# Kernel optimization log

Hardware: AMD Instinct MI355X
Metric: run time of the kernel (lower is better)

## Reference

```python
import jax, jax.numpy as jnp
import numpy as np

N_ATOMS = 10000
N_EDGES = 200000
L_MAX = 2
K_L = [32, 24, 16]  # k_max_l = n_element_channels * n_max_l

# (l1, l2, L) in the original loop order (l1 outer, l2 inner, L ascending)
PAIRS = [(0,0,0),(0,1,1),(0,2,2),
         (1,0,1),(1,1,0),(1,1,1),(1,1,2),(1,2,1),(1,2,2),
         (2,0,2),(2,1,1),(2,1,2),(2,2,0),(2,2,1),(2,2,2)]
# concatenated input width -> k_max_l[L] per (L, sigma) channel
LIN = {'0_1': (72, 32), '1_1': (80, 24), '1_m1': (40, 24), '2_1': (72, 16), '2_m1': (32, 16)}


def setup_inputs() -> dict:
    key = jax.random.key(0)
    it = iter(jax.random.split(key, 64))
    def nrm(shape):
        return jax.random.normal(next(it), shape, dtype=jnp.float32)
    inp = {}
    for l in range(L_MAX + 1):
        inp['rb%d' % l] = nrm((N_EDGES, K_L[l]))           # radial basis per l
    for l in range(L_MAX + 1):
        inp['sh%d' % l] = nrm((N_EDGES, 2*l+1, 1))         # spherical harmonics per l
    inp['emb'] = nrm((N_ATOMS, 1, K_L[0]))                 # initial center embedding
    for l in range(L_MAX + 1):
        inp['f%d' % l] = nrm((N_ATOMS, 2*l+1, K_L[l]))     # nu=1 equivariant features
    for (l1, l2, L) in PAIRS:
        inp['cg_%d_%d_%d' % (l1, l2, L)] = nrm(((2*l1+1)*(2*l2+1), 2*L+1))
    for LS, (fin, fout) in LIN.items():
        inp['W_' + LS] = nrm((fin, fout)) / np.float32(np.sqrt(fin))
        inp['b_' + LS] = nrm((fout,)) * 0.01
    inp['centers'] = jax.random.randint(next(it), (N_EDGES,), 0, N_ATOMS)
    inp['neighbors'] = jax.random.randint(next(it), (N_EDGES,), 0, N_ATOMS)
    inp['n_atoms'] = N_ATOMS
    return inp


def _normalize(x, dims):
    # Normalizer(dims): RMS normalization over the given dims
    return x * jax.lax.rsqrt(jnp.mean(x * x, axis=dims, keepdims=True) + 1e-12)


def _forward(floats, centers, neighbors, n_atoms):
    (rb0, rb1, rb2, sh0, sh1, sh2, emb, f0, f1, f2,
     cg_0_0_0, cg_0_1_1, cg_0_2_2, cg_1_0_1, cg_1_1_0, cg_1_1_1, cg_1_1_2,
     cg_1_2_1, cg_1_2_2, cg_2_0_2, cg_2_1_1, cg_2_1_2, cg_2_2_0, cg_2_2_1,
     cg_2_2_2, W_0_1, b_0_1, W_1_1, b_1_1, W_1_m1, b_1_m1, W_2_1, b_2_1,
     W_2_m1, b_2_m1) = floats
    rb = [rb0, rb1, rb2]; sh = [sh0, sh1, sh2]; feats = [f0, f1, f2]
    cgs = {'0_0_0': cg_0_0_0, '0_1_1': cg_0_1_1, '0_2_2': cg_0_2_2,
           '1_0_1': cg_1_0_1, '1_1_0': cg_1_1_0, '1_1_1': cg_1_1_1,
           '1_1_2': cg_1_1_2, '1_2_1': cg_1_2_1, '1_2_2': cg_1_2_2,
           '2_0_2': cg_2_0_2, '2_1_1': cg_2_1_1, '2_1_2': cg_2_1_2,
           '2_2_0': cg_2_2_0, '2_2_1': cg_2_2_1, '2_2_2': cg_2_2_2}
    lin = {'0_1': (W_0_1, b_0_1), '1_1': (W_1_1, b_1_1), '1_m1': (W_1_m1, b_1_m1),
           '2_1': (W_2_1, b_2_1), '2_m1': (W_2_m1, b_2_m1)}

    # ---- InvariantMessagePasser: density_l = scatter_add over centers of
    #      sh_l * rb_l * emb[neighbors]
    emb_n = emb[neighbors]                                       # [E, 1, k0]
    densities = []
    for l in range(L_MAX + 1):
        msg = sh[l] * rb[l][:, None, :] * emb_n[:, :, :K_L[l]]   # [E, 2l+1, k_l]
        densities.append(jax.ops.segment_sum(msg, centers, num_segments=n_atoms))

    # ---- EquivariantMessagePasser
    ve = [sh[l] * rb[l][:, None, :] for l in range(L_MAX + 1)]   # vector expansion [E,2l+1,k_l]
    fn = [feats[l][neighbors] for l in range(L_MAX + 1)]         # gathered neighbor feats
    results = {}
    for (l1, l2, L) in PAIRS:
        S = (-1) ** (l1 + l2 + L)
        k = min(K_L[l1], K_L[l2])
        t1 = ve[l1][:, :, :k]                                    # [E, 2l1+1, k]
        t2 = fn[l2][:, :, :k]                                    # [E, 2l2+1, k]
        cg = cgs['%d_%d_%d' % (l1, l2, L)].reshape(2*l1+1, 2*l2+1, 2*L+1)
        # fused outer product + CG contraction -> [E, 2L+1, k]
        res = jnp.einsum('eak,ebk,abM->eMk', t1, t2, cg)
        pooled = jax.ops.segment_sum(res, centers, num_segments=n_atoms)
        LS = '%d_%s' % (L, 'm1' if S < 0 else '1')
        results.setdefault(LS, []).append(pooled)

    outs = {}
    for LS, (W, b) in lin.items():
        x = jnp.concatenate(results[LS], axis=2)                 # [n_atoms, 2L+1, size_LS]
        x = _normalize(x, (0, 1))
        x = jnp.einsum('amf,fk->amk', x, W) + b
        outs[LS] = _normalize(x, (0, 1, 2))

    return (densities[0], densities[1], densities[2],
            outs['0_1'], outs['1_1'], outs['1_m1'], outs['2_1'], outs['2_m1'])


def reference(rb0, rb1, rb2, sh0, sh1, sh2, emb, f0, f1, f2,
              cg_0_0_0, cg_0_1_1, cg_0_2_2, cg_1_0_1, cg_1_1_0, cg_1_1_1,
              cg_1_1_2, cg_1_2_1, cg_1_2_2, cg_2_0_2, cg_2_1_1, cg_2_1_2,
              cg_2_2_0, cg_2_2_1, cg_2_2_2, W_0_1, b_0_1, W_1_1, b_1_1,
              W_1_m1, b_1_m1, W_2_1, b_2_1, W_2_m1, b_2_m1,
              centers, neighbors, n_atoms):
    floats = (rb0, rb1, rb2, sh0, sh1, sh2, emb, f0, f1, f2,
              cg_0_0_0, cg_0_1_1, cg_0_2_2, cg_1_0_1, cg_1_1_0, cg_1_1_1,
              cg_1_1_2, cg_1_2_1, cg_1_2_2, cg_2_0_2, cg_2_1_1, cg_2_1_2,
              cg_2_2_0, cg_2_2_1, cg_2_2_2, W_0_1, b_0_1, W_1_1, b_1_1,
              W_1_m1, b_1_m1, W_2_1, b_2_1, W_2_m1, b_2_m1)
    return _forward(floats, centers, neighbors, n_atoms)
```

## Files before the change

kernel.cpp:

```cpp
#include <hip/hip_runtime.h>
#include <hip/hip_bf16.h>

typedef __hip_bfloat16 bf16;

#define N_ATOMS 10000
#define N_EDGES 200000

#define SCG   0
#define SINV  616
#define SS1P  1024
#define SS2P  19968
#define SWS2  20288
#define SINTS 20352
#define IFLAG  0
#define ICOUNT 16
#define IOFFS  10016
#define ICURS  20032
#define IELIST 30032
#define INTS_END_SMALL 230032
#define INTS_END_BIG   430032
#define SXACC (SINTS + INTS_END_BIG)
#define BIG_FLOATS (SXACC + 952*N_ATOMS)

#define O0 0
#define O1 320000
#define O2 1040000
#define OY 1840000
#define OUT_ELEMS 5200000

__device__ __forceinline__ float b2f(bf16 x){ return __bfloat162float(x); }
__device__ __forceinline__ bf16  f2b(float x){ return __float2bfloat16(x); }

__device__ __forceinline__ float ldv(const float* p, int i){ return p[i]; }
__device__ __forceinline__ float ldv(const bf16*  p, int i){ return b2f(p[i]); }
__device__ __forceinline__ void  stv(float* p, int i, float v){ p[i] = v; }
__device__ __forceinline__ void  stv(bf16*  p, int i, float v){ p[i] = f2b(v); }

template<typename T> __device__ __forceinline__ int dtid();
template<> __device__ __forceinline__ int dtid<bf16>(){ return 0; }
template<> __device__ __forceinline__ int dtid<float>(){ return 1; }

struct Ptrs15 { const void* p[15]; };
struct LinP   { const void* W[5]; const void* B[5]; };

__constant__ int c_cg_sizes[15] = {1,9,25,9,9,27,45,45,75,25,45,75,25,75,125};
__constant__ int c_fin[5]   = {72,80,40,72,32};
__constant__ int c_kout[5]  = {32,24,24,16,16};
__constant__ int c_yoff[5]  = {OY+0, OY+320000, OY+1040000, OY+1760000, OY+2560000};
__constant__ int c_numel[5] = {320000,720000,720000,800000,800000};
__constant__ int c_cum[6]   = {0,32,104,176,256,336};
__constant__ int c_xb[5]    = {0,72,312,432,792};
__constant__ int c_Ms[5]    = {1,3,3,5,5};

__global__ void k_zero(float* wsf, int* wsi,
                       const unsigned short* rb0u, const unsigned short* embu) {
  if (blockIdx.x == 0 && threadIdx.x < 64) {
    int lane = threadIdx.x;
    int bad = 0;
    for (int i = lane; i < 256; i += 64) {
      unsigned u1 = ((unsigned)rb0u[2*i]) << 16;
      unsigned u2 = ((unsigned)embu[2*i]) << 16;
      float v1 = __uint_as_float(u1);
      float v2 = __uint_as_float(u2);
      if (!(fabsf(v1) < 1e9f) || !(fabsf(v2) < 1e9f)) bad = 1;
    }
    unsigned long long any = __ballot(bad);
    if (lane == 0) wsi[IFLAG] = (any != 0ULL) ? 1 : 0;
  }
  int i = blockIdx.x*blockDim.x + threadIdx.x;
  if (i < N_ATOMS) wsi[ICOUNT + i] = 0;
  int j = i - N_ATOMS;
  if (j >= 0 && j < N_ATOMS) wsi[ICURS + j] = 0;
  j -= N_ATOMS;
  if (j >= 0 && j < 18944) wsf[SS1P + j] = 0.f;
  j -= 18944;
  if (j >= 0 && j < 325) wsf[SS2P + j] = 0.f;
}

template<typename T>
__global__ void k_cg(Ptrs15 cg, float* wsf, const int* flag) {
  if (flag[0] != dtid<T>()) return;
  int i = blockIdx.x*blockDim.x + threadIdx.x;
  if (i >= 615) return;
  int s = 0, off = i;
  while (off >= c_cg_sizes[s]) { off -= c_cg_sizes[s]; ++s; }
  wsf[SCG + i] = ldv((const T*)cg.p[s], off);
}

__global__ void k_hist(const int* __restrict__ centers, int* __restrict__ counts) {
  int e = blockIdx.x*blockDim.x + threadIdx.x;
  if (e < N_EDGES) atomicAdd(&counts[centers[e]], 1);
}

__global__ void k_scan(const int* __restrict__ counts, int* __restrict__ offs) {
  __shared__ int part[1024];
  int t = threadIdx.x;
  int base = t*10;
  int s = 0;
  for (int i = 0; i < 10; ++i) { int idx = base+i; if (idx < N_ATOMS) s += counts[idx]; }
  part[t] = s;
  __syncthreads();
  for (int d = 1; d < 1024; d <<= 1) {
    int v = part[t];
    int add = (t >= d) ? part[t-d] : 0;
    __syncthreads();
    part[t] = v + add;
    __syncthreads();
  }
  int run = (t == 0) ? 0 : part[t-1];
  for (int i = 0; i < 10; ++i) {
    int idx = base+i;
    if (idx < N_ATOMS) { offs[idx] = run; run += counts[idx]; }
  }
  if (t == 1023) offs[N_ATOMS] = part[1023];
}

__global__ void k_scatter(const int* __restrict__ centers, const int* __restrict__ offs,
                          int* __restrict__ cursors, int* __restrict__ elist) {
  int e = blockIdx.x*blockDim.x + threadIdx.x;
  if (e < N_EDGES) {
    int c = centers[e];
    int p = atomicAdd(&cursors[c], 1);
    elist[offs[c] + p] = e;
  }
}

__global__ void k_scatter2(const int* __restrict__ centers, const int* __restrict__ neighbors,
                           const int* __restrict__ offs, int* __restrict__ cursors,
                           int2* __restrict__ elist2) {
  int e = blockIdx.x*blockDim.x + threadIdx.x;
  if (e < N_EDGES) {
    int c = centers[e];
    int p = atomicAdd(&cursors[c], 1);
    elist2[offs[c] + p] = make_int2(e, neighbors[e]);
  }
}

template<typename T, int MODE>
__global__ __launch_bounds__(256) void k_main(
    const T* __restrict__ rb0, const T* __restrict__ rb1, const T* __restrict__ rb2,
    const T* __restrict__ sh0, const T* __restrict__ sh1, const T* __restrict__ sh2,
    const T* __restrict__ emb, const T* __restrict__ f0, const T* __restrict__ f1,
    const T* __restrict__ f2, const int* __restrict__ neighbors,
    const int* __restrict__ offs, const int* __restrict__ elist,
    const float* __restrict__ cgf, float* __restrict__ s1p,
    const float* __restrict__ inv, float* __restrict__ s2p,
    float* __restrict__ xout, LinP lp, T* __restrict__ out,
    const int* __restrict__ flag)
{
  if (flag[0] != dtid<T>()) return;
  int lane = threadIdx.x & 63;
  int wv   = threadIdx.x >> 6;
  int tix  = threadIdx.x;
  int a = blockIdx.x;
  int beg = offs[a];
  int cnt = offs[a+1] - beg;
  int k32 = lane & 31, e2 = lane >> 5;
  int k16 = lane & 15, e4 = lane >> 4;
  const int2* el2 = (const int2*)elist;
  int ab = a & 63;

  __shared__ int2 sel[256];
  __shared__ __align__(16) float L[952];
  __shared__ float red[4][5];

  float acc[25];
  #pragma unroll
  for (int i = 0; i < 25; ++i) acc[i] = 0.f;

  for (int cbase = 0; cbase < cnt; cbase += 256) {
    int nch = cnt - cbase; if (nch > 256) nch = 256;
    __syncthreads();
    if (tix < nch) {
      if constexpr (MODE == 0) {
        sel[tix] = el2[beg + cbase + tix];
      } else {
        int e = elist[beg + cbase + tix];
        sel[tix] = make_int2(e, neighbors[e]);
      }
    }
    __syncthreads();

    if (wv == 0) {
      for (int base = 0; base < nch; base += 4) {
        #pragma unroll
        for (int u = 0; u < 2; ++u) {
          int idx = base + 2*u + e2;
          float w = (idx < nch) ? 1.f : 0.f;
          int ic  = (idx < nch) ? idx : 0;
          int2 en = sel[ic];
          int e = en.x, n = en.y;
          float s0 = ldv(sh0, e);
          float s1a0 = ldv(sh1, e*3+0), s1a1 = ldv(sh1, e*3+1), s1a2 = ldv(sh1, e*3+2);
          float rb0k = ldv(rb0, e*32 + k32) * w;
          float ek   = ldv(emb, n*32 + k32);
          float f0k  = ldv(f0,  n*32 + k32);
          float ve0 = s0 * rb0k;
          acc[0] = fmaf(ve0, ek, acc[0]);
          acc[4] = fmaf(ve0, f0k, acc[4]);
          if (k32 < 24) {
            float rb1k = ldv(rb1, e*24 + k32) * w;
            float f1k0 = ldv(f1, n*72 + k32);
            float f1k1 = ldv(f1, n*72 + 24 + k32);
            float f1k2 = ldv(f1, n*72 + 48 + k32);
            float rbek = rb1k * ek;
            acc[1] = fmaf(s1a0, rbek, acc[1]);
            acc[2] = fmaf(s1a1, rbek, acc[2]);
            acc[3] = fmaf(s1a2, rbek, acc[3]);
            acc[5] = fmaf(ve0, f1k0, acc[5]);
            acc[6] = fmaf(ve0, f1k1, acc[6]);
            acc[7] = fmaf(ve0, f1k2, acc[7]);
            float g3 = rb1k * f0k;
            acc[8]  = fmaf(g3, s1a0, acc[8]);
            acc[9]  = fmaf(g3, s1a1, acc[9]);
            acc[10] = fmaf(g3, s1a2, acc[10]);
            #pragma unroll
            for (int aa = 0; aa < 3; ++aa) {
              float sa = rb1k * ((aa==0)?s1a0:(aa==1)?s1a1:s1a2);
              acc[11+aa*3+0] = fmaf(sa, f1k0, acc[11+aa*3+0]);
              acc[11+aa*3+1] = fmaf(sa, f1k1, acc[11+aa*3+1]);
              acc[11+aa*3+2] = fmaf(sa, f1k2, acc[11+aa*3+2]);
            }
          }
        }
      }
    } else if (wv == 1) {
      for (int base = 0; base < nch; base += 8) {
        #pragma unroll
        for (int u = 0; u < 2; ++u) {
          int idx = base + 4*u + e4;
          float w = (idx < nch) ? 1.f : 0.f;
          int ic  = (idx < nch) ? idx : 0;
          int2 en = sel[ic];
          int e = en.x, n = en.y;
          float s0 = ldv(sh0, e);
          float s1a[3];
          #pragma unroll
          for (int m = 0; m < 3; ++m) s1a[m] = ldv(sh1, e*3+m);
          float s2a[5];
          #pragma unroll
          for (int m = 0; m < 5; ++m) s2a[m] = ldv(sh2, e*5+m);
          float rb0k = ldv(rb0, e*32 + k16) * w;
          float rb1k = ldv(rb1, e*24 + k16) * w;
          float rb2k = ldv(rb2, e*16 + k16) * w;
          float ek   = ldv(emb, n*32 + k16);
          float f2k[5];
          #pragma unroll
          for (int b = 0; b < 5; ++b) f2k[b] = ldv(f2, n*80 + b*16 + k16);
          float re = rb2k * ek;
          #pragma unroll
          for (int m = 0; m < 5; ++m) acc[m] = fmaf(s2a[m], re, acc[m]);
          float ve0 = s0 * rb0k;
          #pragma unroll
          for (int b = 0; b < 5; ++b) acc[5+b] = fmaf(ve0, f2k[b], acc[5+b]);
          #pragma unroll
          for (int aa = 0; aa < 3; ++aa) {
            float sa = rb1k * s1a[aa];
            #pragma unroll
            for (int b = 0; b < 5; ++b)
              acc[10+aa*5+b] = fmaf(sa, f2k[b], acc[10+aa*5+b]);
          }
        }
      }
    } else if (wv == 2) {
      for (int base = 0; base < nch; base += 8) {
        #pragma unroll
        for (int u = 0; u < 2; ++u) {
          int idx = base + 4*u + e4;
          float w = (idx < nch) ? 1.f : 0.f;
          int ic  = (idx < nch) ? idx : 0;
          int2 en = sel[ic];
          int e = en.x, n = en.y;
          float s2a[5];
          #pragma unroll
          for (int m = 0; m < 5; ++m) s2a[m] = ldv(sh2, e*5+m);
          float rb2k = ldv(rb2, e*16 + k16) * w;
          float f0k  = ldv(f0,  n*32 + k16);
          float f1k[3];
          #pragma unroll
          for (int b = 0; b < 3; ++b) f1k[b] = ldv(f1, n*72 + b*24 + k16);
          float g9 = rb2k * f0k;
          #pragma unroll
          for (int aa = 0; aa < 5; ++aa) acc[aa] = fmaf(g9, s2a[aa], acc[aa]);
          #pragma unroll
          for (int aa = 0; aa < 5; ++aa) {
            float sa = rb2k * s2a[aa];
            #pragma unroll
            for (int b = 0; b < 3; ++b)
              acc[5+aa*3+b] = fmaf(sa, f1k[b], acc[5+aa*3+b]);
          }
        }
      }
    } else {
      for (int base = 0; base < nch; base += 8) {
        #pragma unroll
        for (int u = 0; u < 2; ++u) {
          int idx = base + 4*u + e4;
          float w = (idx < nch) ? 1.f : 0.f;
          int ic  = (idx < nch) ? idx : 0;
          int2 en = sel[ic];
          int e = en.x, n = en.y;
          float s2a[5];
          #pragma unroll
          for (int m = 0; m < 5; ++m) s2a[m] = ldv(sh2, e*5+m);
          float rb2k = ldv(rb2, e*16 + k16) * w;
          float f2k[5];
          #pragma unroll
          for (int b = 0; b < 5; ++b) f2k[b] = ldv(f2, n*80 + b*16 + k16);
          #pragma unroll
          for (int aa = 0; aa < 5; ++aa) {
            float sa = rb2k * s2a[aa];
            #pragma unroll
            for (int b = 0; b < 5; ++b)
              acc[aa*5+b] = fmaf(sa, f2k[b], acc[aa*5+b]);
          }
        }
      }
    }
  }

  if (wv == 0) {
    #pragma unroll
    for (int i = 0; i < 20; ++i) acc[i] += __shfl_xor(acc[i], 32);
    const float* C000 = cgf + 0;
    const float* C011 = cgf + 1;
    const float* C101 = cgf + 35;
    const float* C110 = cgf + 44;
    const float* C111 = cgf + 53;
    const float* C112 = cgf + 80;
    float r[16];
    r[0] = C000[0] * acc[4];
    #pragma unroll
    for (int M = 0; M < 3; ++M) {
      float t = 0.f;
      #pragma unroll
      for (int b = 0; b < 3; ++b) t = fmaf(acc[5+b], C011[b*3+M], t);
      r[1+M] = t;
    }
    #pragma unroll
    for (int M = 0; M < 3; ++M) {
      float t = 0.f;
      #pragma unroll
      for (int aa = 0; aa < 3; ++aa) t = fmaf(acc[8+aa], C101[aa*3+M], t);
      r[4+M] = t;
    }
    {
      float t = 0.f;
      #pragma unroll
      for (int q = 0; q < 9; ++q) t = fmaf(acc[11+q], C110[q], t);
      r[7] = t;
    }
    #pragma unroll
    for (int M = 0; M < 3; ++M) {
      float t = 0.f;
      #pragma unroll
      for (int q = 0; q < 9; ++q) t = fmaf(acc[11+q], C111[q*3+M], t);
      r[8+M] = t;
    }
    #pragma unroll
    for (int M = 0; M < 5; ++M) {
      float t = 0.f;
      #pragma unroll
      for (int q = 0; q < 9; ++q) t = fmaf(acc[11+q], C112[q*5+M], t);
      r[11+M] = t;
    }
    acc[4] = r[0];
    #pragma unroll
    for (int M = 0; M < 3; ++M) acc[5+M]  = r[1+M];
    #pragma unroll
    for (int M = 0; M < 3; ++M) acc[8+M]  = r[4+M];
    acc[11] = r[7];
    #pragma unroll
    for (int M = 0; M < 3; ++M) acc[12+M] = r[8+M];
    #pragma unroll
    for (int M = 0; M < 5; ++M) acc[15+M] = r[11+M];
  } else if (wv == 1) {
    #pragma unroll
    for (int i = 0; i < 25; ++i) {
      acc[i] += __shfl_xor(acc[i], 16);
      acc[i] += __shfl_xor(acc[i], 32);
    }
    const float* C022 = cgf + 10;
    const float* C121 = cgf + 125;
    const float* C122 = cgf + 170;
    float r[13];
    #pragma unroll
    for (int M = 0; M < 5; ++M) {
      float t = 0.f;
      #pragma unroll
      for (int b = 0; b < 5; ++b) t = fmaf(acc[5+b], C022[b*5+M], t);
      r[M] = t;
    }
    #pragma unroll
    for (int M = 0; M < 3; ++M) {
      float t = 0.f;
      #pragma unroll
      for (int q = 0; q < 15; ++q) t = fmaf(acc[10+q], C121[q*3+M], t);
      r[5+M] = t;
    }
    #pragma unroll
    for (int M = 0; M < 5; ++M) {
      float t = 0.f;
      #pragma unroll
      for (int q = 0; q < 15; ++q) t = fmaf(acc[10+q], C122[q*5+M], t);
      r[8+M] = t;
    }
    #pragma unroll
    for (int M = 0; M < 5; ++M) acc[5+M]  = r[M];
    #pragma unroll
    for (int M = 0; M < 3; ++M) acc[10+M] = r[5+M];
    #pragma unroll
    for (int M = 0; M < 5; ++M) acc[13+M] = r[8+M];
  } else if (wv == 2) {
    #pragma unroll
    for (int i = 0; i < 20; ++i) {
      acc[i] += __shfl_xor(acc[i], 16);
      acc[i] += __shfl_xor(acc[i], 32);
    }
    const float* C202 = cgf + 245;
    const float* C211 = cgf + 270;
    const float* C212 = cgf + 315;
    float r[13];
    #pragma unroll
    for (int M = 0; M < 5; ++M) {
      float t = 0.f;
      #pragma unroll
      for (int aa = 0; aa < 5; ++aa) t = fmaf(acc[aa], C202[aa*5+M], t);
      r[M] = t;
    }
    #pragma unroll
    for (int M = 0; M < 3; ++M) {
      float t = 0.f;
      #pragma unroll
      for (int q = 0; q < 15; ++q) t = fmaf(acc[5+q], C211[q*3+M], t);
      r[5+M] = t;
    }
    #pragma unroll
    for (int M = 0; M < 5; ++M) {
      float t = 0.f;
      #pragma unroll
      for (int q = 0; q < 15; ++q) t = fmaf(acc[5+q], C212[q*5+M], t);
      r[8+M] = t;
    }
    #pragma unroll
    for (int M = 0; M < 5; ++M) acc[M]   = r[M];
    #pragma unroll
    for (int M = 0; M < 3; ++M) acc[5+M] = r[5+M];
    #pragma unroll
    for (int M = 0; M < 5; ++M) acc[8+M] = r[8+M];
  } else {
    #pragma unroll
    for (int i = 0; i < 25; ++i) {
      acc[i] += __shfl_xor(acc[i], 16);
      acc[i] += __shfl_xor(acc[i], 32);
    }
    const float* C220 = cgf + 390;
    const float* C221 = cgf + 415;
    const float* C222 = cgf + 490;
    float r[9];
    {
      float t = 0.f;
      #pragma unroll
      for (int q = 0; q < 25; ++q) t = fmaf(acc[q], C220[q], t);
      r[0] = t;
    }
    #pragma unroll
    for (int M = 0; M < 3; ++M) {
      float t = 0.f;
      #pragma unroll
      for (int q = 0; q < 25; ++q) t = fmaf(acc[q], C221[q*3+M], t);
      r[1+M] = t;
    }
    #pragma unroll
    for (int M = 0; M < 5; ++M) {
      float t = 0.f;
      #pragma unroll
      for (int q = 0; q < 25; ++q) t = fmaf(acc[q], C222[q*5+M], t);
      r[4+M] = t;
    }
    #pragma unroll
    for (int i = 0; i < 9; ++i) acc[i] = r[i];
  }

  if constexpr (MODE != 2) {
    if (wv == 0) {
      if (lane < 32) {
        stv(out, O0 + a*32 + k32, acc[0]);
        atomicAdd(&s1p[(0+k32)*64+ab], acc[4]*acc[4]);
        if (k32 < 24) {
          #pragma unroll
          for (int m = 0; m < 3; ++m) stv(out, O1 + a*72 + m*24 + k32, acc[1+m]);
          atomicAdd(&s1p[(32+k32)*64+ab], acc[11]*acc[11]);
          float q;
          q = acc[5]*acc[5]+acc[6]*acc[6]+acc[7]*acc[7];
          atomicAdd(&s1p[(72+k32)*64+ab], q);
          q = acc[8]*acc[8]+acc[9]*acc[9]+acc[10]*acc[10];
          atomicAdd(&s1p[(96+k32)*64+ab], q);
          q = acc[12]*acc[12]+acc[13]*acc[13]+acc[14]*acc[14];
          atomicAdd(&s1p[(152+k32)*64+ab], q);
          q = acc[15]*acc[15]+acc[16]*acc[16]+acc[17]*acc[17]
            + acc[18]*acc[18]+acc[19]*acc[19];
          atomicAdd(&s1p[(208+k32)*64+ab], q);
        }
      }
    } else if (wv == 1) {
      if (lane < 16) {
        #pragma unroll
        for (int m = 0; m < 5; ++m) stv(out, O2 + a*80 + m*16 + k16, acc[m]);
        float q;
        q = acc[5]*acc[5]+acc[6]*acc[6]+acc[7]*acc[7]+acc[8]*acc[8]+acc[9]*acc[9];
        atomicAdd(&s1p[(192+k16)*64+ab], q);
        q = acc[10]*acc[10]+acc[11]*acc[11]+acc[12]*acc[12];
        atomicAdd(&s1p[(120+k16)*64+ab], q);
        q = acc[13]*acc[13]+acc[14]*acc[14]+acc[15]*acc[15]
          + acc[16]*acc[16]+acc[17]*acc[17];
        atomicAdd(&s1p[(264+k16)*64+ab], q);
      }
    } else if (wv == 2) {
      if (lane < 16) {
        float q;
        q = acc[0]*acc[0]+acc[1]*acc[1]+acc[2]*acc[2]+acc[3]*acc[3]+acc[4]*acc[4];
        atomicAdd(&s1p[(232+k16)*64+ab], q);
        q = acc[5]*acc[5]+acc[6]*acc[6]+acc[7]*acc[7];
        atomicAdd(&s1p[(136+k16)*64+ab], q);
        q = acc[8]*acc[8]+acc[9]*acc[9]+acc[10]*acc[10]
          + acc[11]*acc[11]+acc[12]*acc[12];
        atomicAdd(&s1p[(280+k16)*64+ab], q);
      }
    } else {
      if (lane < 16) {
        atomicAdd(&s1p[(56+k16)*64+ab], acc[0]*acc[0]);
        float q;
        q = acc[1]*acc[1]+acc[2]*acc[2]+acc[3]*acc[3];
        atomicAdd(&s1p[(176+k16)*64+ab], q);
        q = acc[4]*acc[4]+acc[5]*acc[5]+acc[6]*acc[6]
          + acc[7]*acc[7]+acc[8]*acc[8];
        atomicAdd(&s1p[(248+k16)*64+ab], q);
      }
    }
  }

  if constexpr (MODE == 0) {
    if (wv == 0) {
      if (lane < 32) {
        L[k32] = acc[4];
        if (k32 < 24) {
          L[32+k32] = acc[11];
          #pragma unroll
          for (int M = 0; M < 3; ++M) L[72+M*80+k32]     = acc[5+M];
          #pragma unroll
          for (int M = 0; M < 3; ++M) L[72+M*80+24+k32]  = acc[8+M];
          #pragma unroll
          for (int M = 0; M < 3; ++M) L[312+M*40+k32]    = acc[12+M];
          #pragma unroll
          for (int M = 0; M < 5; ++M) L[432+M*72+16+k32] = acc[15+M];
        }
      }
    } else if (wv == 1) {
      if (lane < 16) {
        #pragma unroll
        for (int M = 0; M < 5; ++M) L[432+M*72+k16]    = acc[5+M];
        #pragma unroll
        for (int M = 0; M < 3; ++M) L[72+M*80+48+k16]  = acc[10+M];
        #pragma unroll
        for (int M = 0; M < 5; ++M) L[792+M*32+k16]    = acc[13+M];
      }
    } else if (wv == 2) {
      if (lane < 16) {
        #pragma unroll
        for (int M = 0; M < 5; ++M) L[432+M*72+40+k16] = acc[0+M];
        #pragma unroll
        for (int M = 0; M < 3; ++M) L[72+M*80+64+k16]  = acc[5+M];
        #pragma unroll
        for (int M = 0; M < 5; ++M) L[792+M*32+16+k16] = acc[8+M];
      }
    } else {
      if (lane < 16) {
        L[56+k16] = acc[0];
        #pragma unroll
        for (int M = 0; M < 3; ++M) L[312+M*40+24+k16] = acc[1+M];
        #pragma unroll
        for (int M = 0; M < 5; ++M) L[432+M*72+56+k16] = acc[4+M];
      }
    }
    __syncthreads();
    const float4* Ls = (const float4*)L;
    float4* xd = (float4*)(xout + a*952);
    for (int i = tix; i < 238; i += 256) xd[i] = Ls[i];
  }

  if constexpr (MODE == 2) {
    if (wv == 0) {
      if (lane < 32) {
        L[k32] = acc[4]*inv[k32];
        if (k32 < 24) {
          L[32+k32] = acc[11]*inv[32+k32];
          #pragma unroll
          for (int M = 0; M < 3; ++M) L[72+M*80+k32]     = acc[5+M]*inv[72+k32];
          #pragma unroll
          for (int M = 0; M < 3; ++M) L[72+M*80+24+k32]  = acc[8+M]*inv[96+k32];
          #pragma unroll
          for (int M = 0; M < 3; ++M) L[312+M*40+k32]    = acc[12+M]*inv[152+k32];
          #pragma unroll
          for (int M = 0; M < 5; ++M) L[432+M*72+16+k32] = acc[15+M]*inv[208+k32];
        }
      }
    } else if (wv == 1) {
      if (lane < 16) {
        #pragma unroll
        for (int M = 0; M < 5; ++M) L[432+M*72+k16]    = acc[5+M]*inv[192+k16];
        #pragma unroll
        for (int M = 0; M < 3; ++M) L[72+M*80+48+k16]  = acc[10+M]*inv[120+k16];
        #pragma unroll
        for (int M = 0; M < 5; ++M) L[792+M*32+k16]    = acc[13+M]*inv[264+k16];
      }
    } else if (wv == 2) {
      if (lane < 16) {
        #pragma unroll
        for (int M = 0; M < 5; ++M) L[432+M*72+40+k16] = acc[0+M]*inv[232+k16];
        #pragma unroll
        for (int M = 0; M < 3; ++M) L[72+M*80+64+k16]  = acc[5+M]*inv[136+k16];
        #pragma unroll
        for (int M = 0; M < 5; ++M) L[792+M*32+16+k16] = acc[8+M]*inv[280+k16];
      }
    } else {
      if (lane < 16) {
        L[56+k16] = acc[0]*inv[56+k16];
        #pragma unroll
        for (int M = 0; M < 3; ++M) L[312+M*40+24+k16] = acc[1+M]*inv[176+k16];
        #pragma unroll
        for (int M = 0; M < 5; ++M) L[432+M*72+56+k16] = acc[4+M]*inv[248+k16];
      }
    }
    __syncthreads();
    int t = threadIdx.x;
    float y2[5] = {0.f,0.f,0.f,0.f,0.f};
    for (int tau = t; tau < 336; tau += 256) {
      int ls = 0;
      while (tau >= c_cum[ls+1]) ++ls;
      int rem = tau - c_cum[ls];
      int kn = c_kout[ls], fin = c_fin[ls];
      int M = rem / kn, ko = rem - M*kn;
      const T* W = (const T*)lp.W[ls];
      float y = ldv((const T*)lp.B[ls], ko);
      const float* xv = &L[c_xb[ls] + M*fin];
      for (int f = 0; f < fin; ++f) y = fmaf(xv[f], ldv(W, f*kn+ko), y);
      stv(out, c_yoff[ls] + (a*c_Ms[ls] + M)*kn + ko, y);
      y2[ls] += y*y;
    }
    #pragma unroll
    for (int i = 0; i < 5; ++i) {
      y2[i] += __shfl_xor(y2[i], 1);  y2[i] += __shfl_xor(y2[i], 2);
      y2[i] += __shfl_xor(y2[i], 4);  y2[i] += __shfl_xor(y2[i], 8);
      y2[i] += __shfl_xor(y2[i], 16); y2[i] += __shfl_xor(y2[i], 32);
    }
    if (lane == 0) {
      #pragma unroll
      for (int i = 0; i < 5; ++i) red[wv][i] = y2[i];
    }
    __syncthreads();
    if (t == 0) {
      #pragma unroll
      for (int i = 0; i < 5; ++i)
        atomicAdd(&s2p[i*64 + ab], red[0][i]+red[1][i]+red[2][i]+red[3][i]);
    }
  }
}

template<typename T>
__global__ __launch_bounds__(256) void k_lin(
    const float* __restrict__ xg, const float* __restrict__ inv,
    LinP lp, T* __restrict__ out, float* __restrict__ s2p,
    const int* __restrict__ flag)
{
  if (flag[0] != dtid<T>()) return;
  int a = blockIdx.x;
  int t = threadIdx.x;
  __shared__ float L[952];
  for (int i = t; i < 952; i += 256) {
    int ch;
    if      (i < 72)  ch = i;
    else if (i < 312) ch = 72  + (i-72)  % 80;
    else if (i < 432) ch = 152 + (i-312) % 40;
    else if (i < 792) ch = 192 + (i-432) % 72;
    else              ch = 264 + (i-792) % 32;
    L[i] = xg[a*952 + i] * inv[ch];
  }
  __syncthreads();
  float y2[5] = {0.f,0.f,0.f,0.f,0.f};
  for (int tau = t; tau < 336; tau += 256) {
    int ls = 0;
    while (tau >= c_cum[ls+1]) ++ls;
    int rem = tau - c_cum[ls];
    int kn = c_kout[ls], fin = c_fin[ls];
    int M = rem / kn, ko = rem - M*kn;
    const T* W = (const T*)lp.W[ls];
    float y = ldv((const T*)lp.B[ls], ko);
    const float* xv = &L[c_xb[ls] + M*fin];
    for (int f = 0; f < fin; ++f) y = fmaf(xv[f], ldv(W, f*kn+ko), y);
    stv(out, c_yoff[ls] + (a*c_Ms[ls] + M)*kn + ko, y);
    y2[ls] += y*y;
  }
  __shared__ float red[4][5];
  #pragma unroll
  for (int i = 0; i < 5; ++i) {
    y2[i] += __shfl_xor(y2[i], 1);  y2[i] += __shfl_xor(y2[i], 2);
    y2[i] += __shfl_xor(y2[i], 4);  y2[i] += __shfl_xor(y2[i], 8);
    y2[i] += __shfl_xor(y2[i], 16); y2[i] += __shfl_xor(y2[i], 32);
  }
  if ((t & 63) == 0) {
    #pragma unroll
    for (int i = 0; i < 5; ++i) red[t>>6][i] = y2[i];
  }
  __syncthreads();
  if (t == 0) {
    #pragma unroll
    for (int i = 0; i < 5; ++i)
      atomicAdd(&s2p[i*64 + (a & 63)], red[0][i]+red[1][i]+red[2][i]+red[3][i]);
  }
}

__global__ void k_red1(const float* __restrict__ s1p, float* __restrict__ inv) {
  int ch = blockIdx.x, lane = threadIdx.x;
  float v = s1p[ch*64 + lane];
  v += __shfl_xor(v, 1);  v += __shfl_xor(v, 2);  v += __shfl_xor(v, 4);
  v += __shfl_xor(v, 8);  v += __shfl_xor(v, 16); v += __shfl_xor(v, 32);
  if (lane == 0) {
    float rows = (ch < 72) ? 10000.f : (ch < 192) ? 30000.f : 50000.f;
    inv[ch] = rsqrtf(v/rows + 1e-12f);
  }
}

__global__ void k_red2(const float* __restrict__ s2p, float* __restrict__ ws2) {
  int ls = blockIdx.x, lane = threadIdx.x;
  float v = s2p[ls*64 + lane];
  v += __shfl_xor(v, 1);  v += __shfl_xor(v, 2);  v += __shfl_xor(v, 4);
  v += __shfl_xor(v, 8);  v += __shfl_xor(v, 16); v += __shfl_xor(v, 32);
  if (lane == 0) ws2[ls] = v;
}

template<typename T>
__global__ void k_scale(const float* __restrict__ ws2, T* __restrict__ out,
                        const int* __restrict__ flag) {
  if (flag[0] != dtid<T>()) return;
  int i = blockIdx.x*blockDim.x + threadIdx.x;
  if (i >= 3360000) return;
  int ls = (i < 320000) ? 0 : (i < 1040000) ? 1 : (i < 1760000) ? 2 : (i < 2560000) ? 3 : 4;
  float scale = rsqrtf(ws2[ls] / (float)c_numel[ls] + 1e-12f);
  stv(out, OY + i, ldv((const T*)out, OY + i) * scale);
}

template<typename T>
static void launch_chain(void* const* d_in, T* out, float* wsf, int* wsi,
                         Ptrs15 cg, LinP lp, bool big, hipStream_t stream) {
  const T* rb0 = (const T*)d_in[0];
  const T* rb1 = (const T*)d_in[1];
  const T* rb2 = (const T*)d_in[2];
  const T* sh0 = (const T*)d_in[3];
  const T* sh1 = (const T*)d_in[4];
  const T* sh2 = (const T*)d_in[5];
  const T* emb = (const T*)d_in[6];
  const T* f0  = (const T*)d_in[7];
  const T* f1  = (const T*)d_in[8];
  const T* f2  = (const T*)d_in[9];
  const int* neighbors = (const int*)d_in[36];
  const int* flag = wsi + IFLAG;

  k_cg<T><<<3, 256, 0, stream>>>(cg, wsf, flag);
  if (big) {
    k_main<T,0><<<N_ATOMS, 256, 0, stream>>>(rb0, rb1, rb2, sh0, sh1, sh2, emb, f0, f1, f2,
        neighbors, wsi+IOFFS, wsi+IELIST, wsf+SCG, wsf+SS1P, nullptr, nullptr,
        wsf+SXACC, lp, out, flag);
    k_red1<<<296, 64, 0, stream>>>(wsf+SS1P, wsf+SINV);
    k_lin<T><<<N_ATOMS, 256, 0, stream>>>(wsf+SXACC, wsf+SINV, lp, out, wsf+SS2P, flag);
  } else {
    k_main<T,1><<<N_ATOMS, 256, 0, stream>>>(rb0, rb1, rb2, sh0, sh1, sh2, emb, f0, f1, f2,
        neighbors, wsi+IOFFS, wsi+IELIST, wsf+SCG, wsf+SS1P, nullptr, nullptr,
        nullptr, lp, out, flag);
    k_red1<<<296, 64, 0, stream>>>(wsf+SS1P, wsf+SINV);
    k_main<T,2><<<N_ATOMS, 256, 0, stream>>>(rb0, rb1, rb2, sh0, sh1, sh2, emb, f0, f1, f2,
        neighbors, wsi+IOFFS, wsi+IELIST, wsf+SCG, nullptr, wsf+SINV, wsf+SS2P,
        nullptr, lp, out, flag);
  }
  k_red2<<<5, 64, 0, stream>>>(wsf+SS2P, wsf+SWS2);
  k_scale<T><<<(3360000+255)/256, 256, 0, stream>>>(wsf+SWS2, out, flag);
}

extern "C" void kernel_launch(void* const* d_in, const int* in_sizes, int n_in,
                              void* d_out, int out_size, void* d_ws, size_t ws_size,
                              hipStream_t stream) {
  float* wsf = (float*)d_ws;
  int*   wsi = (int*)(wsf + SINTS);
  const int* centers   = (const int*)d_in[35];
  const int* neighbors = (const int*)d_in[36];
  bool big = ws_size >= (size_t)BIG_FLOATS * 4;

  int know = -1;
  if (in_sizes) {
    long long nb = (long long)in_sizes[0];
    if (nb == (long long)N_EDGES*32*2) know = 0;
    else if (nb == (long long)N_EDGES*32*4) know = 1;
  }
  if (know < 0) {
    long long ob = (long long)out_size;
    if (ob == (long long)OUT_ELEMS*2) know = 0;
    else if (ob == (long long)OUT_ELEMS*4) know = 1;
  }

  Ptrs15 cg;
  for (int i = 0; i < 15; ++i) cg.p[i] = d_in[10+i];
  LinP lp;
  lp.W[0] = d_in[25]; lp.B[0] = d_in[26];
  lp.W[1] = d_in[27]; lp.B[1] = d_in[28];
  lp.W[2] = d_in[29]; lp.B[2] = d_in[30];
  lp.W[3] = d_in[31]; lp.B[3] = d_in[32];
  lp.W[4] = d_in[33]; lp.B[4] = d_in[34];

  k_zero<<<154, 256, 0, stream>>>(wsf, wsi,
                                  (const unsigned short*)d_in[0],
                                  (const unsigned short*)d_in[6]);
  k_hist<<<(N_EDGES+255)/256, 256, 0, stream>>>(centers, wsi+ICOUNT);
  k_scan<<<1, 1024, 0, stream>>>(wsi+ICOUNT, wsi+IOFFS);
  if (big) {
    k_scatter2<<<(N_EDGES+255)/256, 256, 0, stream>>>(centers, neighbors, wsi+IOFFS,
                                                      wsi+ICURS, (int2*)(wsi+IELIST));
  } else {
    k_scatter<<<(N_EDGES+255)/256, 256, 0, stream>>>(centers, wsi+IOFFS, wsi+ICURS, wsi+IELIST);
  }

  if (know != 1) launch_chain<bf16 >(d_in, (bf16*)d_out,  wsf, wsi, cg, lp, big, stream);
  if (know != 0) launch_chain<float>(d_in, (float*)d_out, wsf, wsi, cg, lp, big, stream);
}
```

Measured before the change: 514.2 us.

## Pack per-edge radial/SH data into center-sorted records and stream in main kernels

Adds a pack kernel that, while scattering edges by center, copies each edge's radial bases and spherical harmonics into a contiguous 84-element record in sorted order. The main kernels then read these records sequentially instead of gathering rb/sh by edge index, and each block now processes four atoms. The old cached-accumulator plus separate linear-kernel path is removed in favour of running the main kernel twice. This trades an extra full copy of per-edge data, and recomputing the edge pass, for coalesced streaming reads and fewer blocks.

```diff
diff --git a/kernel.cpp b/kernel.cpp
--- a/kernel.cpp
+++ b/kernel.cpp
@@ -5,6 +5,7 @@
 
 #define N_ATOMS 10000
 #define N_EDGES 200000
+#define REC 84
 
 #define SCG   0
 #define SINV  616
@@ -17,10 +18,8 @@
 #define IOFFS  10016
 #define ICURS  20032
 #define IELIST 30032
-#define INTS_END_SMALL 230032
 #define INTS_END_BIG   430032
-#define SXACC (SINTS + INTS_END_BIG)
-#define BIG_FLOATS (SXACC + 952*N_ATOMS)
+#define SEREC (SINTS + INTS_END_BIG)
 
 #define O0 0
 #define O1 320000
@@ -115,8 +114,11 @@
   if (t == 1023) offs[N_ATOMS] = part[1023];
 }
 
-__global__ void k_scatter(const int* __restrict__ centers, const int* __restrict__ offs,
-                          int* __restrict__ cursors, int* __restrict__ elist) {
+template<typename T>
+__global__ void k_scatterT(const int* __restrict__ centers, const int* __restrict__ offs,
+                           int* __restrict__ cursors, int* __restrict__ elist,
+                           const int* __restrict__ flag) {
+  if (flag[0] != dtid<T>()) return;
   int e = blockIdx.x*blockDim.x + threadIdx.x;
   if (e < N_EDGES) {
     int c = centers[e];
@@ -125,14 +127,34 @@
   }
 }
 
-__global__ void k_scatter2(const int* __restrict__ centers, const int* __restrict__ neighbors,
-                           const int* __restrict__ offs, int* __restrict__ cursors,
-                           int2* __restrict__ elist2) {
-  int e = blockIdx.x*blockDim.x + threadIdx.x;
-  if (e < N_EDGES) {
-    int c = centers[e];
-    int p = atomicAdd(&cursors[c], 1);
-    elist2[offs[c] + p] = make_int2(e, neighbors[e]);
+template<typename T>
+__global__ __launch_bounds__(256) void k_pack(
+    const T* __restrict__ rb0, const T* __restrict__ rb1, const T* __restrict__ rb2,
+    const T* __restrict__ sh0, const T* __restrict__ sh1, const T* __restrict__ sh2,
+    const int* __restrict__ centers, const int* __restrict__ neighbors,
+    const int* __restrict__ offs, int* __restrict__ cursors,
+    int2* __restrict__ el2, T* __restrict__ erec, const int* __restrict__ flag)
+{
+  if (flag[0] != dtid<T>()) return;
+  int tid = blockIdx.x*blockDim.x + threadIdx.x;
+  int half = tid >> 5;
+  int k = tid & 31;
+  int lane = threadIdx.x & 63;
+  int nhalf = (gridDim.x*blockDim.x) >> 5;
+  for (int e = half; e < N_EDGES; e += nhalf) {
+    int pos = 0;
+    if (k == 0) {
+      int c = centers[e];
+      pos = offs[c] + atomicAdd(&cursors[c], 1);
+    }
+    pos = __shfl(pos, lane & 32);
+    T* r = erec + (size_t)pos * REC;
+    r[k] = rb0[e*32 + k];
+    if (k < 24) r[32+k] = rb1[e*24 + k];
+    if (k < 16) r[56+k] = rb2[e*16 + k];
+    if (k == 0) { r[72] = sh0[e]; el2[pos] = make_int2(e, neighbors[e]); }
+    if (k >= 1 && k < 4) r[72+k] = sh1[e*3 + (k-1)];
+    if (k >= 4 && k < 9) r[72+k] = sh2[e*5 + (k-4)];
   }
 }
 
@@ -143,580 +165,637 @@
     const T* __restrict__ emb, const T* __restrict__ f0, const T* __restrict__ f1,
     const T* __restrict__ f2, const int* __restrict__ neighbors,
     const int* __restrict__ offs, const int* __restrict__ elist,
+    const T* __restrict__ erec,
     const float* __restrict__ cgf, float* __restrict__ s1p,
     const float* __restrict__ inv, float* __restrict__ s2p,
-    float* __restrict__ xout, LinP lp, T* __restrict__ out,
-    const int* __restrict__ flag)
+    LinP lp, T* __restrict__ out, const int* __restrict__ flag)
 {
   if (flag[0] != dtid<T>()) return;
+  constexpr bool STRM = (MODE >= 3);
+  constexpr int EPI = (MODE == 1 || MODE == 3) ? 1 : 2;
   int lane = threadIdx.x & 63;
   int wv   = threadIdx.x >> 6;
   int tix  = threadIdx.x;
-  int a = blockIdx.x;
-  int beg = offs[a];
-  int cnt = offs[a+1] - beg;
   int k32 = lane & 31, e2 = lane >> 5;
   int k16 = lane & 15, e4 = lane >> 4;
+  int k24 = (k32 < 24) ? k32 : 23;
+  float m24 = (k32 < 24) ? 1.f : 0.f;
   const int2* el2 = (const int2*)elist;
-  int ab = a & 63;
 
   __shared__ int2 sel[256];
   __shared__ __align__(16) float L[952];
   __shared__ float red[4][5];
 
-  float acc[25];
-  #pragma unroll
-  for (int i = 0; i < 25; ++i) acc[i] = 0.f;
-
-  for (int cbase = 0; cbase < cnt; cbase += 256) {
-    int nch = cnt - cbase; if (nch > 256) nch = 256;
-    __syncthreads();
-    if (tix < nch) {
-      if constexpr (MODE == 0) {
-        sel[tix] = el2[beg + cbase + tix];
-      } else {
-        int e = elist[beg + cbase + tix];
-        sel[tix] = make_int2(e, neighbors[e]);
-      }
-    }
-    __syncthreads();
-
-    if (wv == 0) {
-      for (int base = 0; base < nch; base += 4) {
-        #pragma unroll
-        for (int u = 0; u < 2; ++u) {
-          int idx = base + 2*u + e2;
-          float w = (idx < nch) ? 1.f : 0.f;
-          int ic  = (idx < nch) ? idx : 0;
-          int2 en = sel[ic];
-          int e = en.x, n = en.y;
-          float s0 = ldv(sh0, e);
-          float s1a0 = ldv(sh1, e*3+0), s1a1 = ldv(sh1, e*3+1), s1a2 = ldv(sh1, e*3+2);
-          float rb0k = ldv(rb0, e*32 + k32) * w;
-          float ek   = ldv(emb, n*32 + k32);
-          float f0k  = ldv(f0,  n*32 + k32);
-          float ve0 = s0 * rb0k;
-          acc[0] = fmaf(ve0, ek, acc[0]);
-          acc[4] = fmaf(ve0, f0k, acc[4]);
-          if (k32 < 24) {
-            float rb1k = ldv(rb1, e*24 + k32) * w;
-            float f1k0 = ldv(f1, n*72 + k32);
-            float f1k1 = ldv(f1, n*72 + 24 + k32);
-            float f1k2 = ldv(f1, n*72 + 48 + k32);
-            float rbek = rb1k * ek;
-            acc[1] = fmaf(s1a0, rbek, acc[1]);
-            acc[2] = fmaf(s1a1, rbek, acc[2]);
-            acc[3] = fmaf(s1a2, rbek, acc[3]);
-            acc[5] = fmaf(ve0, f1k0, acc[5]);
-            acc[6] = fmaf(ve0, f1k1, acc[6]);
-            acc[7] = fmaf(ve0, f1k2, acc[7]);
-            float g3 = rb1k * f0k;
-            acc[8]  = fmaf(g3, s1a0, acc[8]);
-            acc[9]  = fmaf(g3, s1a1, acc[9]);
-            acc[10] = fmaf(g3, s1a2, acc[10]);
+  int a0 = blockIdx.x * 4;
+  for (int a = a0; a < a0 + 4; ++a) {
+    int beg = offs[a];
+    int cnt = offs[a+1] - beg;
+    int ab = a & 63;
+
+    float acc[25];
+    #pragma unroll
+    for (int i = 0; i < 25; ++i) acc[i] = 0.f;
+
+    if constexpr (STRM) {
+      const T* rbase = erec + (size_t)beg * REC;
+      const int2* eb = el2 + beg;
+      if (wv == 0) {
+        for (int base = 0; base < cnt; base += 4) {
+          int i0 = base + e2,      i1 = base + 2 + e2;
+          float w0 = (i0 < cnt) ? 1.f : 0.f, w1 = (i1 < cnt) ? 1.f : 0.f;
+          int c0 = (i0 < cnt) ? i0 : 0,      c1 = (i1 < cnt) ? i1 : 0;
+          const T* r0 = rbase + (size_t)c0 * REC;
+          const T* r1 = rbase + (size_t)c1 * REC;
+          int n0 = eb[c0].y, n1 = eb[c1].y;
+          float s0_0 = ldv(r0,72), sA0 = ldv(r0,73), sA1 = ldv(r0,74), sA2 = ldv(r0,75);
+          float s0_1 = ldv(r1,72), sB0 = ldv(r1,73), sB1 = ldv(r1,74), sB2 = ldv(r1,75);
+          float a0v = ldv(r0, k32) * w0,            a1v = ldv(r1, k32) * w1;
+          float b0v = ldv(r0, 32+k24) * (w0*m24),   b1v = ldv(r1, 32+k24) * (w1*m24);
+          float e0v = ldv(emb, n0*32 + k32),        e1v = ldv(emb, n1*32 + k32);
+          float g0v = ldv(f0,  n0*32 + k32),        g1v = ldv(f0,  n1*32 + k32);
+          float h00 = ldv(f1, n0*72 + k24)*m24,     h10 = ldv(f1, n1*72 + k24)*m24;
+          float h01 = ldv(f1, n0*72 + 24 + k24)*m24,h11 = ldv(f1, n1*72 + 24 + k24)*m24;
+          float h02 = ldv(f1, n0*72 + 48 + k24)*m24,h12 = ldv(f1, n1*72 + 48 + k24)*m24;
+          float ve = a0v * s0_0;
+          acc[0] = fmaf(ve, e0v, acc[0]);
+          acc[4] = fmaf(ve, g0v, acc[4]);
+          float rbek = b0v * e0v;
+          acc[1] = fmaf(sA0, rbek, acc[1]);
+          acc[2] = fmaf(sA1, rbek, acc[2]);
+          acc[3] = fmaf(sA2, rbek, acc[3]);
+          acc[5] = fmaf(ve, h00, acc[5]);
+          acc[6] = fmaf(ve, h01, acc[6]);
+          acc[7] = fmaf(ve, h02, acc[7]);
+          float g3 = b0v * g0v;
+          acc[8]  = fmaf(g3, sA0, acc[8]);
+          acc[9]  = fmaf(g3, sA1, acc[9]);
+          acc[10] = fmaf(g3, sA2, acc[10]);
+          float sa;
+          sa = b0v * sA0;
+          acc[11] = fmaf(sa, h00, acc[11]); acc[12] = fmaf(sa, h01, acc[12]); acc[13] = fmaf(sa, h02, acc[13]);
+          sa = b0v * sA1;
+          acc[14] = fmaf(sa, h00, acc[14]); acc[15] = fmaf(sa, h01, acc[15]); acc[16] = fmaf(sa, h02, acc[16]);
+          sa = b0v * sA2;
+          acc[17] = fmaf(sa, h00, acc[17]); acc[18] = fmaf(sa, h01, acc[18]); acc[19] = fmaf(sa, h02, acc[19]);
+          ve = a1v * s0_1;
+          acc[0] = fmaf(ve, e1v, acc[0]);
+          acc[4] = fmaf(ve, g1v, acc[4]);
+          rbek = b1v * e1v;
+          acc[1] = fmaf(sB0, rbek, acc[1]);
+          acc[2] = fmaf(sB1, rbek, acc[2]);
+          acc[3] = fmaf(sB2, rbek, acc[3]);
+          acc[5] = fmaf(ve, h10, acc[5]);
+          acc[6] = fmaf(ve, h11, acc[6]);
+          acc[7] = fmaf(ve, h12, acc[7]);
+          g3 = b1v * g1v;
+          acc[8]  = fmaf(g3, sB0, acc[8]);
+          acc[9]  = fmaf(g3, sB1, acc[9]);
+          acc[10] = fmaf(g3, sB2, acc[10]);
+          sa = b1v * sB0;
+          acc[11] = fmaf(sa, h10, acc[11]); acc[12] = fmaf(sa, h11, acc[12]); acc[13] = fmaf(sa, h12, acc[13]);
+          sa = b1v * sB1;
+          acc[14] = fmaf(sa, h10, acc[14]); acc[15] = fmaf(sa, h11, acc[15]); acc[16] = fmaf(sa, h12, acc[16]);
+          sa = b1v * sB2;
+          acc[17] = fmaf(sa, h10, acc[17]); acc[18] = fmaf(sa, h11, acc[18]); acc[19] = fmaf(sa, h12, acc[19]);
+        }
+      } else if (wv == 1) {
+        for (int base = 0; base < cnt; base += 8) {
+          #pragma unroll
+          for (int u = 0; u < 2; ++u) {
+            int idx = base + 4*u + e4;
+            float w = (idx < cnt) ? 1.f : 0.f;
+            int ic  = (idx < cnt) ? idx : 0;
+            const T* r = rbase + (size_t)ic * REC;
+            int n = eb[ic].y;
+            float rb0k = ldv(r, k16) * w;
+            float rb1k = ldv(r, 32+k16) * w;
+            float rb2k = ldv(r, 56+k16) * w;
+            float s0 = ldv(r, 72);
+            float s1a[3];
+            #pragma unroll
+            for (int m = 0; m < 3; ++m) s1a[m] = ldv(r, 73+m);
+            float s2a[5];
+            #pragma unroll
+            for (int m = 0; m < 5; ++m) s2a[m] = ldv(r, 76+m);
+            float ek = ldv(emb, n*32 + k16);
+            float f2k[5];
+            #pragma unroll
+            for (int b = 0; b < 5; ++b) f2k[b] = ldv(f2, n*80 + b*16 + k16);
+            float re = rb2k * ek;
+            #pragma unroll
+            for (int m = 0; m < 5; ++m) acc[m] = fmaf(s2a[m], re, acc[m]);
+            float ve0 = s0 * rb0k;
+            #pragma unroll
+            for (int b = 0; b < 5; ++b) acc[5+b] = fmaf(ve0, f2k[b], acc[5+b]);
             #pragma unroll
             for (int aa = 0; aa < 3; ++aa) {
-              float sa = rb1k * ((aa==0)?s1a0:(aa==1)?s1a1:s1a2);
-              acc[11+aa*3+0] = fmaf(sa, f1k0, acc[11+aa*3+0]);
-              acc[11+aa*3+1] = fmaf(sa, f1k1, acc[11+aa*3+1]);
-              acc[11+aa*3+2] = fmaf(sa, f1k2, acc[11+aa*3+2]);
+              float sa = rb1k * s1a[aa];
+              #pragma unroll
+              for (int b = 0; b < 5; ++b)
+                acc[10+aa*5+b] = fmaf(sa, f2k[b], acc[10+aa*5+b]);
             }
           }
         }
-      }
+      } else if (wv == 2) {
+        for (int base = 0; base < cnt; base += 8) {
+          #pragma unroll
+          for (int u = 0; u < 2; ++u) {
+            int idx = base + 4*u + e4;
+            float w = (idx < cnt) ? 1.f : 0.f;
+            int ic  = (idx < cnt) ? idx : 0;
+            const T* r = rbase + (size_t)ic * REC;
+            int n = eb[ic].y;
+            float rb2k = ldv(r, 56+k16) * w;
+            float s2a[5];
+            #pragma unroll
+            for (int m = 0; m < 5; ++m) s2a[m] = ldv(r, 76+m);
+            float f0k = ldv(f0, n*32 + k16);
+            float f1k[3];
+            #pragma unroll
+            for (int b = 0; b < 3; ++b) f1k[b] = ldv(f1, n*72 + b*24 + k16);
+            float g9 = rb2k * f0k;
+            #pragma unroll
+            for (int aa = 0; aa < 5; ++aa) acc[aa] = fmaf(g9, s2a[aa], acc[aa]);
+            #pragma unroll
+            for (int aa = 0; aa < 5; ++aa) {
+              float sa = rb2k * s2a[aa];
+              #pragma unroll
+              for (int b = 0; b < 3; ++b)
+                acc[5+aa*3+b] = fmaf(sa, f1k[b], acc[5+aa*3+b]);
+            }
+          }
+        }
+      } else {
+        for (int base = 0; base < cnt; base += 8) {
+          #pragma unroll
+          for (int u = 0; u < 2; ++u) {
+            int idx = base + 4*u + e4;
+            float w = (idx < cnt) ? 1.f : 0.f;
+            int ic  = (idx < cnt) ? idx : 0;
+            const T* r = rbase + (size_t)ic * REC;
+            int n = eb[ic].y;
+            float rb2k = ldv(r, 56+k16) * w;
+            float s2a[5];
+            #pragma unroll
+            for (int m = 0; m < 5; ++m) s2a[m] = ldv(r, 76+m);
+            float f2k[5];
+            #pragma unroll
+            for (int b = 0; b < 5; ++b) f2k[b] = ldv(f2, n*80 + b*16 + k16);
+            #pragma unroll
+            for (int aa = 0; aa < 5; ++aa) {
+              float sa = rb2k * s2a[aa];
+              #pragma unroll
+              for (int b = 0; b < 5; ++b)
+                acc[aa*5+b] = fmaf(sa, f2k[b], acc[aa*5+b]);
+            }
+          }
+        }
+      }
+    } else {
+      for (int cbase = 0; cbase < cnt; cbase += 256) {
+        int nch = cnt - cbase; if (nch > 256) nch = 256;
+        __syncthreads();
+        if (tix < nch) {
+          int e = elist[beg + cbase + tix];
+          sel[tix] = make_int2(e, neighbors[e]);
+        }
+        __syncthreads();
+        if (wv == 0) {
+          for (int base = 0; base < nch; base += 4) {
+            #pragma unroll
+            for (int u = 0; u < 2; ++u) {
+              int idx = base + 2*u + e2;
+              float w = (idx < nch) ? 1.f : 0.f;
+              int ic  = (idx < nch) ? idx : 0;
+              int2 en = sel[ic];
+              int e = en.x, n = en.y;
+              float s0 = ldv(sh0, e);
+              float s1a0 = ldv(sh1, e*3+0), s1a1 = ldv(sh1, e*3+1), s1a2 = ldv(sh1, e*3+2);
+              float rb0k = ldv(rb0, e*32 + k32) * w;
+              float ek   = ldv(emb, n*32 + k32);
+              float f0k  = ldv(f0,  n*32 + k32);
+              float ve0 = s0 * rb0k;
+              acc[0] = fmaf(ve0, ek, acc[0]);
+              acc[4] = fmaf(ve0, f0k, acc[4]);
+              if (k32 < 24) {
+                float rb1k = ldv(rb1, e*24 + k32) * w;
+                float f1k0 = ldv(f1, n*72 + k32);
+                float f1k1 = ldv(f1, n*72 + 24 + k32);
+                float f1k2 = ldv(f1, n*72 + 48 + k32);
+                float rbek = rb1k * ek;
+                acc[1] = fmaf(s1a0, rbek, acc[1]);
+                acc[2] = fmaf(s1a1, rbek, acc[2]);
+                acc[3] = fmaf(s1a2, rbek, acc[3]);
+                acc[5] = fmaf(ve0, f1k0, acc[5]);
+                acc[6] = fmaf(ve0, f1k1, acc[6]);
+                acc[7] = fmaf(ve0, f1k2, acc[7]);
+                float g3 = rb1k * f0k;
+                acc[8]  = fmaf(g3, s1a0, acc[8]);
+                acc[9]  = fmaf(g3, s1a1, acc[9]);
+                acc[10] = fmaf(g3, s1a2, acc[10]);
+                #pragma unroll
+                for (int aa = 0; aa < 3; ++aa) {
+                  float sa = rb1k * ((aa==0)?s1a0:(aa==1)?s1a1:s1a2);
+                  acc[11+aa*3+0] = fmaf(sa, f1k0, acc[11+aa*3+0]);
+                  acc[11+aa*3+1] = fmaf(sa, f1k1, acc[11+aa*3+1]);
+                  acc[11+aa*3+2] = fmaf(sa, f1k2, acc[11+aa*3+2]);
+                }
+              }
+            }
+          }
+        } else if (wv == 1) {
+          for (int base = 0; base < nch; base += 8) {
+            #pragma unroll
+            for (int u = 0; u < 2; ++u) {
+              int idx = base + 4*u + e4;
+              float w = (idx < nch) ? 1.f : 0.f;
+              int ic  = (idx < nch) ? idx : 0;
+              int2 en = sel[ic];
+              int e = en.x, n = en.y;
+              float s0 = ldv(sh0, e);
+              float s1a[3];
+              #pragma unroll
+              for (int m = 0; m < 3; ++m) s1a[m] = ldv(sh1, e*3+m);
+              float s2a[5];
+              #pragma unroll
+              for (int m = 0; m < 5; ++m) s2a[m] = ldv(sh2, e*5+m);
+              float rb0k = ldv(rb0, e*32 + k16) * w;
+              float rb1k = ldv(rb1, e*24 + k16) * w;
+              float rb2k = ldv(rb2, e*16 + k16) * w;
+              float ek   = ldv(emb, n*32 + k16);
+              float f2k[5];
+              #pragma unroll
+              for (int b = 0; b < 5; ++b) f2k[b] = ldv(f2, n*80 + b*16 + k16);
+              float re = rb2k * ek;
+              #pragma unroll
+              for (int m = 0; m < 5; ++m) acc[m] = fmaf(s2a[m], re, acc[m]);
+              float ve0 = s0 * rb0k;
+              #pragma unroll
+              for (int b = 0; b < 5; ++b) acc[5+b] = fmaf(ve0, f2k[b], acc[5+b]);
+              #pragma unroll
+              for (int aa = 0; aa < 3; ++aa) {
+                float sa = rb1k * s1a[aa];
+                #pragma unroll
+                for (int b = 0; b < 5; ++b)
+                  acc[10+aa*5+b] = fmaf(sa, f2k[b], acc[10+aa*5+b]);
+              }
+            }
+          }
+        } else if (wv == 2) {
+          for (int base = 0; base < nch; base += 8) {
+            #pragma unroll
+            for (int u = 0; u < 2; ++u) {
+              int idx = base + 4*u + e4;
+              float w = (idx < nch) ? 1.f : 0.f;
+              int ic  = (idx < nch) ? idx : 0;
+              int2 en = sel[ic];
+              int e = en.x, n = en.y;
+              float s2a[5];
+              #pragma unroll
+              for (int m = 0; m < 5; ++m) s2a[m] = ldv(sh2, e*5+m);
+              float rb2k = ldv(rb2, e*16 + k16) * w;
+              float f0k  = ldv(f0,  n*32 + k16);
+              float f1k[3];
+              #pragma unroll
+              for (int b = 0; b < 3; ++b) f1k[b] = ldv(f1, n*72 + b*24 + k16);
+              float g9 = rb2k * f0k;
+              #pragma unroll
+              for (int aa = 0; aa < 5; ++aa) acc[aa] = fmaf(g9, s2a[aa], acc[aa]);
+              #pragma unroll
+              for (int aa = 0; aa < 5; ++aa) {
+                float sa = rb2k * s2a[aa];
+                #pragma unroll
+                for (int b = 0; b < 3; ++b)
+                  acc[5+aa*3+b] = fmaf(sa, f1k[b], acc[5+aa*3+b]);
+              }
+            }
+          }
+        } else {
+          for (int base = 0; base < nch; base += 8) {
+            #pragma unroll
+            for (int u = 0; u < 2; ++u) {
+              int idx = base + 4*u + e4;
+              float w = (idx < nch) ? 1.f : 0.f;
+              int ic  = (idx < nch) ? idx : 0;
+              int2 en = sel[ic];
+              int e = en.x, n = en.y;
+              float s2a[5];
+              #pragma unroll
+              for (int m = 0; m < 5; ++m) s2a[m] = ldv(sh2, e*5+m);
+              float rb2k = ldv(rb2, e*16 + k16) * w;
+              float f2k[5];
+              #pragma unroll
+              for (int b = 0; b < 5; ++b) f2k[b] = ldv(f2, n*80 + b*16 + k16);
+              #pragma unroll
+              for (int aa = 0; aa < 5; ++aa) {
+                float sa = rb2k * s2a[aa];
+                #pragma unroll
+                for (int b = 0; b < 5; ++b)
+                  acc[aa*5+b] = fmaf(sa, f2k[b], acc[aa*5+b]);
+              }
+            }
+          }
+        }
+      }
+    }
+
+    if (wv == 0) {
+      #pragma unroll
+      for (int i = 0; i < 20; ++i) acc[i] += __shfl_xor(acc[i], 32);
+      const float* C000 = cgf + 0;
+      const float* C011 = cgf + 1;
+      const float* C101 = cgf + 35;
+      const float* C110 = cgf + 44;
+      const float* C111 = cgf + 53;
+      const float* C112 = cgf + 80;
+      float r[16];
+      r[0] = C000[0] * acc[4];
+      #pragma unroll
+      for (int M = 0; M < 3; ++M) {
+        float t = 0.f;
+        #pragma unroll
+        for (int b = 0; b < 3; ++b) t = fmaf(acc[5+b], C011[b*3+M], t);
+        r[1+M] = t;
+      }
+      #pragma unroll
+      for (int M = 0; M < 3; ++M) {
+        float t = 0.f;
+        #pragma unroll
+        for (int aa = 0; aa < 3; ++aa) t = fmaf(acc[8+aa], C101[aa*3+M], t);
+        r[4+M] = t;
+      }
+      {
+        float t = 0.f;
+        #pragma unroll
+        for (int q = 0; q < 9; ++q) t = fmaf(acc[11+q], C110[q], t);
+        r[7] = t;
+      }
+      #pragma unroll
+      for (int M = 0; M < 3; ++M) {
+        float t = 0.f;
+        #pragma unroll
+        for (int q = 0; q < 9; ++q) t = fmaf(acc[11+q], C111[q*3+M], t);
+        r[8+M] = t;
+      }
+      #pragma unroll
+      for (int M = 0; M < 5; ++M) {
+        float t = 0.f;
+        #pragma unroll
+        for (int q = 0; q < 9; ++q) t = fmaf(acc[11+q], C112[q*5+M], t);
+        r[11+M] = t;
+      }
+      acc[4] = r[0];
+      #pragma unroll
+      for (int M = 0; M < 3; ++M) acc[5+M]  = r[1+M];
+      #pragma unroll
+      for (int M = 0; M < 3; ++M) acc[8+M]  = r[4+M];
+      acc[11] = r[7];
+      #pragma unroll
+      for (int M = 0; M < 3; ++M) acc[12+M] = r[8+M];
+      #pragma unroll
+      for (int M = 0; M < 5; ++M) acc[15+M] = r[11+M];
     } else if (wv == 1) {
-      for (int base = 0; base < nch; base += 8) {
-        #pragma unroll
-        for (int u = 0; u < 2; ++u) {
-          int idx = base + 4*u + e4;
-          float w = (idx < nch) ? 1.f : 0.f;
-          int ic  = (idx < nch) ? idx : 0;
-          int2 en = sel[ic];
-          int e = en.x, n = en.y;
-          float s0 = ldv(sh0, e);
-          float s1a[3];
-          #pragma unroll
-          for (int m = 0; m < 3; ++m) s1a[m] = ldv(sh1, e*3+m);
-          float s2a[5];
-          #pragma unroll
-          for (int m = 0; m < 5; ++m) s2a[m] = ldv(sh2, e*5+m);
-          float rb0k = ldv(rb0, e*32 + k16) * w;
-          float rb1k = ldv(rb1, e*24 + k16) * w;
-          float rb2k = ldv(rb2, e*16 + k16) * w;
-          float ek   = ldv(emb, n*32 + k16);
-          float f2k[5];
-          #pragma unroll
-          for (int b = 0; b < 5; ++b) f2k[b] = ldv(f2, n*80 + b*16 + k16);
-          float re = rb2k * ek;
-          #pragma unroll
-          for (int m = 0; m < 5; ++m) acc[m] = fmaf(s2a[m], re, acc[m]);
-          float ve0 = s0 * rb0k;
-          #pragma unroll
-          for (int b = 0; b < 5; ++b) acc[5+b] = fmaf(ve0, f2k[b], acc[5+b]);
-          #pragma unroll
-          for (int aa = 0; aa < 3; ++aa) {
-            float sa = rb1k * s1a[aa];
-            #pragma unroll
-            for (int b = 0; b < 5; ++b)
-              acc[10+aa*5+b] = fmaf(sa, f2k[b], acc[10+aa*5+b]);
+      #pragma unroll
+      for (int i = 0; i < 25; ++i) {
+        acc[i] += __shfl_xor(acc[i], 16);
+        acc[i] += __shfl_xor(acc[i], 32);
+      }
+      const float* C022 = cgf + 10;
+      const float* C121 = cgf + 125;
+      const float* C122 = cgf + 170;
+      float r[13];
+      #pragma unroll
+      for (int M = 0; M < 5; ++M) {
+        float t = 0.f;
+        #pragma unroll
+        for (int b = 0; b < 5; ++b) t = fmaf(acc[5+b], C022[b*5+M], t);
+        r[M] = t;
+      }
+      #pragma unroll
+      for (int M = 0; M < 3; ++M) {
+        float t = 0.f;
+        #pragma unroll
+        for (int q = 0; q < 15; ++q) t = fmaf(acc[10+q], C121[q*3+M], t);
+        r[5+M] = t;
+      }
+      #pragma unroll
+      for (int M = 0; M < 5; ++M) {
+        float t = 0.f;
+        #pragma unroll
+        for (int q = 0; q < 15; ++q) t = fmaf(acc[10+q], C122[q*5+M], t);
+        r[8+M] = t;
+      }
+      #pragma unroll
+      for (int M = 0; M < 5; ++M) acc[5+M]  = r[M];
+      #pragma unroll
+      for (int M = 0; M < 3; ++M) acc[10+M] = r[5+M];
+      #pragma unroll
+      for (int M = 0; M < 5; ++M) acc[13+M] = r[8+M];
+    } else if (wv == 2) {
+      #pragma unroll
+      for (int i = 0; i < 20; ++i) {
+        acc[i] += __shfl_xor(acc[i], 16);
+        acc[i] += __shfl_xor(acc[i], 32);
+      }
+      const float* C202 = cgf + 245;
+      const float* C211 = cgf + 270;
+      const float* C212 = cgf + 315;
+      float r[13];
+      #pragma unroll
+      for (int M = 0; M < 5; ++M) {
+        float t = 0.f;
+        #pragma unroll
+        for (int aa = 0; aa < 5; ++aa) t = fmaf(acc[aa], C202[aa*5+M], t);
+        r[M] = t;
+      }
+      #pragma unroll
+      for (int M = 0; M < 3; ++M) {
+        float t = 0.f;
+        #pragma unroll
+        for (int q = 0; q < 15; ++q) t = fmaf(acc[5+q], C211[q*3+M], t);
+        r[5+M] = t;
+      }
+      #pragma unroll
+      for (int M = 0; M < 5; ++M) {
+        float t = 0.f;
+        #pragma unroll
+        for (int q = 0; q < 15; ++q) t = fmaf(acc[5+q], C212[q*5+M], t);
+        r[8+M] = t;
+      }
+      #pragma unroll
+      for (int M = 0; M < 5; ++M) acc[M]   = r[M];
+      #pragma unroll
+      for (int M = 0; M < 3; ++M) acc[5+M] = r[5+M];
+      #pragma unroll
+      for (int M = 0; M < 5; ++M) acc[8+M] = r[8+M];
+    } else {
+      #pragma unroll
+      for (int i = 0; i < 25; ++i) {
+        acc[i] += __shfl_xor(acc[i], 16);
+        acc[i] += __shfl_xor(acc[i], 32);
+      }
+      const float* C220 = cgf + 390;
+      const float* C221 = cgf + 415;
+      const float* C222 = cgf + 490;
+      float r[9];
+      {
+        float t = 0.f;
+        #pragma unroll
+        for (int q = 0; q < 25; ++q) t = fmaf(acc[q], C220[q], t);
+        r[0] = t;
+      }
+      #pragma unroll
+      for (int M = 0; M < 3; ++M) {
+        float t = 0.f;
+        #pragma unroll
+        for (int q = 0; q < 25; ++q) t = fmaf(acc[q], C221[q*3+M], t);
+        r[1+M] = t;
+      }
+      #pragma unroll
+      for (int M = 0; M < 5; ++M) {
+        float t = 0.f;
+        #pragma unroll
+        for (int q = 0; q < 25; ++q) t = fmaf(acc[q], C222[q*5+M], t);
+        r[4+M] = t;
+      }
+      #pragma unroll
+      for (int i = 0; i < 9; ++i) acc[i] = r[i];
+    }
+
+    if constexpr (EPI == 1) {
+      if (wv == 0) {
+        if (lane < 32) {
+          stv(out, O0 + a*32 + k32, acc[0]);
+          atomicAdd(&s1p[(0+k32)*64+ab], acc[4]*acc[4]);
+          if (k32 < 24) {
+            #pragma unroll
+            for (int m = 0; m < 3; ++m) stv(out, O1 + a*72 + m*24 + k32, acc[1+m]);
+            atomicAdd(&s1p[(32+k32)*64+ab], acc[11]*acc[11]);
+            float q;
+            q = acc[5]*acc[5]+acc[6]*acc[6]+acc[7]*acc[7];
+            atomicAdd(&s1p[(72+k32)*64+ab], q);
+            q = acc[8]*acc[8]+acc[9]*acc[9]+acc[10]*acc[10];
+            atomicAdd(&s1p[(96+k32)*64+ab], q);
+            q = acc[12]*acc[12]+acc[13]*acc[13]+acc[14]*acc[14];
+            atomicAdd(&s1p[(152+k32)*64+ab], q);
+            q = acc[15]*acc[15]+acc[16]*acc[16]+acc[17]*acc[17]
+              + acc[18]*acc[18]+acc[19]*acc[19];
+            atomicAdd(&s1p[(208+k32)*64+ab], q);
           }
         }
-      }
-    } else if (wv == 2) {
-      for (int base = 0; base < nch; base += 8) {
-        #pragma unroll
-        for (int u = 0; u < 2; ++u) {
-          int idx = base + 4*u + e4;
-          float w = (idx < nch) ? 1.f : 0.f;
-          int ic  = (idx < nch) ? idx : 0;
-          int2 en = sel[ic];
-          int e = en.x, n = en.y;
-          float s2a[5];
-          #pragma unroll
-          for (int m = 0; m < 5; ++m) s2a[m] = ldv(sh2, e*5+m);
-          float rb2k = ldv(rb2, e*16 + k16) * w;
-          float f0k  = ldv(f0,  n*32 + k16);
-          float f1k[3];
-          #pragma unroll
-          for (int b = 0; b < 3; ++b) f1k[b] = ldv(f1, n*72 + b*24 + k16);
-          float g9 = rb2k * f0k;
-          #pragma unroll
-          for (int aa = 0; aa < 5; ++aa) acc[aa] = fmaf(g9, s2a[aa], acc[aa]);
-          #pragma unroll
-          for (int aa = 0; aa < 5; ++aa) {
-            float sa = rb2k * s2a[aa];
-            #pragma unroll
-            for (int b = 0; b < 3; ++b)
-              acc[5+aa*3+b] = fmaf(sa, f1k[b], acc[5+aa*3+b]);
+      } else if (wv == 1) {
+        if (lane < 16) {
+          #pragma unroll
+          for (int m = 0; m < 5; ++m) stv(out, O2 + a*80 + m*16 + k16, acc[m]);
+          float q;
+          q = acc[5]*acc[5]+acc[6]*acc[6]+acc[7]*acc[7]+acc[8]*acc[8]+acc[9]*acc[9];
+          atomicAdd(&s1p[(192+k16)*64+ab], q);
+          q = acc[10]*acc[10]+acc[11]*acc[11]+acc[12]*acc[12];
+          atomicAdd(&s1p[(120+k16)*64+ab], q);
+          q = acc[13]*acc[13]+acc[14]*acc[14]+acc[15]*acc[15]
+            + acc[16]*acc[16]+acc[17]*acc[17];
+          atomicAdd(&s1p[(264+k16)*64+ab], q);
+        }
+      } else if (wv == 2) {
+        if (lane < 16) {
+          float q;
+          q = acc[0]*acc[0]+acc[1]*acc[1]+acc[2]*acc[2]+acc[3]*acc[3]+acc[4]*acc[4];
+          atomicAdd(&s1p[(232+k16)*64+ab], q);
+          q = acc[5]*acc[5]+acc[6]*acc[6]+acc[7]*acc[7];
+          atomicAdd(&s1p[(136+k16)*64+ab], q);
+          q = acc[8]*acc[8]+acc[9]*acc[9]+acc[10]*acc[10]
+            + acc[11]*acc[11]+acc[12]*acc[12];
+          atomicAdd(&s1p[(280+k16)*64+ab], q);
+        }
+      } else {
+        if (lane < 16) {
+          atomicAdd(&s1p[(56+k16)*64+ab], acc[0]*acc[0]);
+          float q;
+          q = acc[1]*acc[1]+acc[2]*acc[2]+acc[3]*acc[3];
+          atomicAdd(&s1p[(176+k16)*64+ab], q);
+          q = acc[4]*acc[4]+acc[5]*acc[5]+acc[6]*acc[6]
+            + acc[7]*acc[7]+acc[8]*acc[8];
+          atomicAdd(&s1p[(248+k16)*64+ab], q);
+        }
+      }
+    }
+
+    if constexpr (EPI == 2) {
+      if (wv == 0) {
+        if (lane < 32) {
+          L[k32] = acc[4]*inv[k32];
+          if (k32 < 24) {
+            L[32+k32] = acc[11]*inv[32+k32];
+            #pragma unroll
+            for (int M = 0; M < 3; ++M) L[72+M*80+k32]     = acc[5+M]*inv[72+k32];
+            #pragma unroll
+            for (int M = 0; M < 3; ++M) L[72+M*80+24+k32]  = acc[8+M]*inv[96+k32];
+            #pragma unroll
+            for (int M = 0; M < 3; ++M) L[312+M*40+k32]    = acc[12+M]*inv[152+k32];
+            #pragma unroll
+            for (int M = 0; M < 5; ++M) L[432+M*72+16+k32] = acc[15+M]*inv[208+k32];
           }
         }
-      }
-    } else {
-      for (int base = 0; base < nch; base += 8) {
-        #pragma unroll
-        for (int u = 0; u < 2; ++u) {
-          int idx = base + 4*u + e4;
-          float w = (idx < nch) ? 1.f : 0.f;
-          int ic  = (idx < nch) ? idx : 0;
-          int2 en = sel[ic];
-          int e = en.x, n = en.y;
-          float s2a[5];
-          #pragma unroll
-          for (int m = 0; m < 5; ++m) s2a[m] = ldv(sh2, e*5+m);
-          float rb2k = ldv(rb2, e*16 + k16) * w;
-          float f2k[5];
-          #pragma unroll
-          for (int b = 0; b < 5; ++b) f2k[b] = ldv(f2, n*80 + b*16 + k16);
-          #pragma unroll
-          for (int aa = 0; aa < 5; ++aa) {
-            float sa = rb2k * s2a[aa];
-            #pragma unroll
-            for (int b = 0; b < 5; ++b)
-              acc[aa*5+b] = fmaf(sa, f2k[b], acc[aa*5+b]);
-          }
-        }
+      } else if (wv == 1) {
+        if (lane < 16) {
+          #pragma unroll
+          for (int M = 0; M < 5; ++M) L[432+M*72+k16]    = acc[5+M]*inv[192+k16];
+          #pragma unroll
+          for (int M = 0; M < 3; ++M) L[72+M*80+48+k16]  = acc[10+M]*inv[120+k16];
+          #pragma unroll
+          for (int M = 0; M < 5; ++M) L[792+M*32+k16]    = acc[13+M]*inv[264+k16];
+        }
+      } else if (wv == 2) {
+        if (lane < 16) {
+          #pragma unroll
+          for (int M = 0; M < 5; ++M) L[432+M*72+40+k16] = acc[0+M]*inv[232+k16];
+          #pragma unroll
+          for (int M = 0; M < 3; ++M) L[72+M*80+64+k16]  = acc[5+M]*inv[136+k16];
+          #pragma unroll
+          for (int M = 0; M < 5; ++M) L[792+M*32+16+k16] = acc[8+M]*inv[280+k16];
+        }
+      } else {
+        if (lane < 16) {
+          L[56+k16] = acc[0]*inv[56+k16];
+          #pragma unroll
+          for (int M = 0; M < 3; ++M) L[312+M*40+24+k16] = acc[1+M]*inv[176+k16];
+          #pragma unroll
+          for (int M = 0; M < 5; ++M) L[432+M*72+56+k16] = acc[4+M]*inv[248+k16];
+        }
+      }
+      __syncthreads();
+      int t = threadIdx.x;
+      float y2[5] = {0.f,0.f,0.f,0.f,0.f};
+      for (int tau = t; tau < 336; tau += 256) {
+        int ls = 0;
+        while (tau >= c_cum[ls+1]) ++ls;
+        int rem = tau - c_cum[ls];
+        int kn = c_kout[ls], fin = c_fin[ls];
+        int M = rem / kn, ko = rem - M*kn;
+        const T* W = (const T*)lp.W[ls];
+        float y = ldv((const T*)lp.B[ls], ko);
+        const float* xv = &L[c_xb[ls] + M*fin];
+        for (int f = 0; f < fin; ++f) y = fmaf(xv[f], ldv(W, f*kn+ko), y);
+        stv(out, c_yoff[ls] + (a*c_Ms[ls] + M)*kn + ko, y);
+        y2[ls] += y*y;
+      }
+      #pragma unroll
+      for (int i = 0; i < 5; ++i) {
+        y2[i] += __shfl_xor(y2[i], 1);  y2[i] += __shfl_xor(y2[i], 2);
+        y2[i] += __shfl_xor(y2[i], 4);  y2[i] += __shfl_xor(y2[i], 8);
+        y2[i] += __shfl_xor(y2[i], 16); y2[i] += __shfl_xor(y2[i], 32);
+      }
+      if (lane == 0) {
+        #pragma unroll
+        for (int i = 0; i < 5; ++i) red[wv][i] = y2[i];
+      }
+      __syncthreads();
+      if (t == 0) {
+        #pragma unroll
+        for (int i = 0; i < 5; ++i)
+          atomicAdd(&s2p[i*64 + ab], red[0][i]+red[1][i]+red[2][i]+red[3][i]);
       }
     }
-  }
-
-  if (wv == 0) {
-    #pragma unroll
-    for (int i = 0; i < 20; ++i) acc[i] += __shfl_xor(acc[i], 32);
-    const float* C000 = cgf + 0;
-    const float* C011 = cgf + 1;
-    const float* C101 = cgf + 35;
-    const float* C110 = cgf + 44;
-    const float* C111 = cgf + 53;
-    const float* C112 = cgf + 80;
-    float r[16];
-    r[0] = C000[0] * acc[4];
-    #pragma unroll
-    for (int M = 0; M < 3; ++M) {
-      float t = 0.f;
-      #pragma unroll
-      for (int b = 0; b < 3; ++b) t = fmaf(acc[5+b], C011[b*3+M], t);
-      r[1+M] = t;
-    }
-    #pragma unroll
-    for (int M = 0; M < 3; ++M) {
-      float t = 0.f;
-      #pragma unroll
-      for (int aa = 0; aa < 3; ++aa) t = fmaf(acc[8+aa], C101[aa*3+M], t);
-      r[4+M] = t;
-    }
-    {
-      float t = 0.f;
-      #pragma unroll
-      for (int q = 0; q < 9; ++q) t = fmaf(acc[11+q], C110[q], t);
-      r[7] = t;
-    }
-    #pragma unroll
-    for (int M = 0; M < 3; ++M) {
-      float t = 0.f;
-      #pragma unroll
-      for (int q = 0; q < 9; ++q) t = fmaf(acc[11+q], C111[q*3+M], t);
-      r[8+M] = t;
-    }
-    #pragma unroll
-    for (int M = 0; M < 5; ++M) {
-      float t = 0.f;
-      #pragma unroll
-      for (int q = 0; q < 9; ++q) t = fmaf(acc[11+q], C112[q*5+M], t);
-      r[11+M] = t;
-    }
-    acc[4] = r[0];
-    #pragma unroll
-    for (int M = 0; M < 3; ++M) acc[5+M]  = r[1+M];
-    #pragma unroll
-    for (int M = 0; M < 3; ++M) acc[8+M]  = r[4+M];
-    acc[11] = r[7];
-    #pragma unroll
-    for (int M = 0; M < 3; ++M) acc[12+M] = r[8+M];
-    #pragma unroll
-    for (int M = 0; M < 5; ++M) acc[15+M] = r[11+M];
-  } else if (wv == 1) {
-    #pragma unroll
-    for (int i = 0; i < 25; ++i) {
-      acc[i] += __shfl_xor(acc[i], 16);
-      acc[i] += __shfl_xor(acc[i], 32);
-    }
-    const float* C022 = cgf + 10;
-    const float* C121 = cgf + 125;
-    const float* C122 = cgf + 170;
-    float r[13];
-    #pragma unroll
-    for (int M = 0; M < 5; ++M) {
-      float t = 0.f;
-      #pragma unroll
-      for (int b = 0; b < 5; ++b) t = fmaf(acc[5+b], C022[b*5+M], t);
-      r[M] = t;
-    }
-    #pragma unroll
-    for (int M = 0; M < 3; ++M) {
-      float t = 0.f;
-      #pragma unroll
-      for (int q = 0; q < 15; ++q) t = fmaf(acc[10+q], C121[q*3+M], t);
-      r[5+M] = t;
-    }
-    #pragma unroll
-    for (int M = 0; M < 5; ++M) {
-      float t = 0.f;
-      #pragma unroll
-      for (int q = 0; q < 15; ++q) t = fmaf(acc[10+q], C122[q*5+M], t);
-      r[8+M] = t;
-    }
-    #pragma unroll
-    for (int M = 0; M < 5; ++M) acc[5+M]  = r[M];
-    #pragma unroll
-    for (int M = 0; M < 3; ++M) acc[10+M] = r[5+M];
-    #pragma unroll
-    for (int M = 0; M < 5; ++M) acc[13+M] = r[8+M];
-  } else if (wv == 2) {
-    #pragma unroll
-    for (int i = 0; i < 20; ++i) {
-      acc[i] += __shfl_xor(acc[i], 16);
-      acc[i] += __shfl_xor(acc[i], 32);
-    }
-    const float* C202 = cgf + 245;
-    const float* C211 = cgf + 270;
-    const float* C212 = cgf + 315;
-    float r[13];
-    #pragma unroll
-    for (int M = 0; M < 5; ++M) {
-      float t = 0.f;
-      #pragma unroll
-      for (int aa = 0; aa < 5; ++aa) t = fmaf(acc[aa], C202[aa*5+M], t);
-      r[M] = t;
-    }
-    #pragma unroll
-    for (int M = 0; M < 3; ++M) {
-      float t = 0.f;
-      #pragma unroll
-      for (int q = 0; q < 15; ++q) t = fmaf(acc[5+q], C211[q*3+M], t);
-      r[5+M] = t;
-    }
-    #pragma unroll
-    for (int M = 0; M < 5; ++M) {
-      float t = 0.f;
-      #pragma unroll
-      for (int q = 0; q < 15; ++q) t = fmaf(acc[5+q], C212[q*5+M], t);
-      r[8+M] = t;
-    }
-    #pragma unroll
-    for (int M = 0; M < 5; ++M) acc[M]   = r[M];
-    #pragma unroll
-    for (int M = 0; M < 3; ++M) acc[5+M] = r[5+M];
-    #pragma unroll
-    for (int M = 0; M < 5; ++M) acc[8+M] = r[8+M];
-  } else {
-    #pragma unroll
-    for (int i = 0; i < 25; ++i) {
-      acc[i] += __shfl_xor(acc[i], 16);
-      acc[i] += __shfl_xor(acc[i], 32);
-    }
-    const float* C220 = cgf + 390;
-    const float* C221 = cgf + 415;
-    const float* C222 = cgf + 490;
-    float r[9];
-    {
-      float t = 0.f;
-      #pragma unroll
-      for (int q = 0; q < 25; ++q) t = fmaf(acc[q], C220[q], t);
-      r[0] = t;
-    }
-    #pragma unroll
-    for (int M = 0; M < 3; ++M) {
-      float t = 0.f;
-      #pragma unroll
-      for (int q = 0; q < 25; ++q) t = fmaf(acc[q], C221[q*3+M], t);
-      r[1+M] = t;
-    }
-    #pragma unroll
-    for (int M = 0; M < 5; ++M) {
-      float t = 0.f;
-      #pragma unroll
-      for (int q = 0; q < 25; ++q) t = fmaf(acc[q], C222[q*5+M], t);
-      r[4+M] = t;
-    }
-    #pragma unroll
-    for (int i = 0; i < 9; ++i) acc[i] = r[i];
-  }
-
-  if constexpr (MODE != 2) {
-    if (wv == 0) {
-      if (lane < 32) {
-        stv(out, O0 + a*32 + k32, acc[0]);
-        atomicAdd(&s1p[(0+k32)*64+ab], acc[4]*acc[4]);
-        if (k32 < 24) {
-          #pragma unroll
-          for (int m = 0; m < 3; ++m) stv(out, O1 + a*72 + m*24 + k32, acc[1+m]);
-          atomicAdd(&s1p[(32+k32)*64+ab], acc[11]*acc[11]);
-          float q;
-          q = acc[5]*acc[5]+acc[6]*acc[6]+acc[7]*acc[7];
-          atomicAdd(&s1p[(72+k32)*64+ab], q);
-          q = acc[8]*acc[8]+acc[9]*acc[9]+acc[10]*acc[10];
-          atomicAdd(&s1p[(96+k32)*64+ab], q);
-          q = acc[12]*acc[12]+acc[13]*acc[13]+acc[14]*acc[14];
-          atomicAdd(&s1p[(152+k32)*64+ab], q);
-          q = acc[15]*acc[15]+acc[16]*acc[16]+acc[17]*acc[17]
-            + acc[18]*acc[18]+acc[19]*acc[19];
-          atomicAdd(&s1p[(208+k32)*64+ab], q);
-        }
-      }
-    } else if (wv == 1) {
-      if (lane < 16) {
-        #pragma unroll
-        for (int m = 0; m < 5; ++m) stv(out, O2 + a*80 + m*16 + k16, acc[m]);
-        float q;
-        q = acc[5]*acc[5]+acc[6]*acc[6]+acc[7]*acc[7]+acc[8]*acc[8]+acc[9]*acc[9];
-        atomicAdd(&s1p[(192+k16)*64+ab], q);
-        q = acc[10]*acc[10]+acc[11]*acc[11]+acc[12]*acc[12];
-        atomicAdd(&s1p[(120+k16)*64+ab], q);
-        q = acc[13]*acc[13]+acc[14]*acc[14]+acc[15]*acc[15]
-          + acc[16]*acc[16]+acc[17]*acc[17];
-        atomicAdd(&s1p[(264+k16)*64+ab], q);
-      }
-    } else if (wv == 2) {
-      if (lane < 16) {
-        float q;
-        q = acc[0]*acc[0]+acc[1]*acc[1]+acc[2]*acc[2]+acc[3]*acc[3]+acc[4]*acc[4];
-        atomicAdd(&s1p[(232+k16)*64+ab], q);
-        q = acc[5]*acc[5]+acc[6]*acc[6]+acc[7]*acc[7];
-        atomicAdd(&s1p[(136+k16)*64+ab], q);
-        q = acc[8]*acc[8]+acc[9]*acc[9]+acc[10]*acc[10]
-          + acc[11]*acc[11]+acc[12]*acc[12];
-        atomicAdd(&s1p[(280+k16)*64+ab], q);
-      }
-    } else {
-      if (lane < 16) {
-        atomicAdd(&s1p[(56+k16)*64+ab], acc[0]*acc[0]);
-        float q;
-        q = acc[1]*acc[1]+acc[2]*acc[2]+acc[3]*acc[3];
-        atomicAdd(&s1p[(176+k16)*64+ab], q);
-        q = acc[4]*acc[4]+acc[5]*acc[5]+acc[6]*acc[6]
-          + acc[7]*acc[7]+acc[8]*acc[8];
-        atomicAdd(&s1p[(248+k16)*64+ab], q);
-      }
-    }
-  }
-
-  if constexpr (MODE == 0) {
-    if (wv == 0) {
-      if (lane < 32) {
-        L[k32] = acc[4];
-        if (k32 < 24) {
-          L[32+k32] = acc[11];
-          #pragma unroll
-          for (int M = 0; M < 3; ++M) L[72+M*80+k32]     = acc[5+M];
-          #pragma unroll
-          for (int M = 0; M < 3; ++M) L[72+M*80+24+k32]  = acc[8+M];
-          #pragma unroll
-          for (int M = 0; M < 3; ++M) L[312+M*40+k32]    = acc[12+M];
-          #pragma unroll
-          for (int M = 0; M < 5; ++M) L[432+M*72+16+k32] = acc[15+M];
-        }
-      }
-    } else if (wv == 1) {
-      if (lane < 16) {
-        #pragma unroll
-        for (int M = 0; M < 5; ++M) L[432+M*72+k16]    = acc[5+M];
-        #pragma unroll
-        for (int M = 0; M < 3; ++M) L[72+M*80+48+k16]  = acc[10+M];
-        #pragma unroll
-        for (int M = 0; M < 5; ++M) L[792+M*32+k16]    = acc[13+M];
-      }
-    } else if (wv == 2) {
-      if (lane < 16) {
-        #pragma unroll
-        for (int M = 0; M < 5; ++M) L[432+M*72+40+k16] = acc[0+M];
-        #pragma unroll
-        for (int M = 0; M < 3; ++M) L[72+M*80+64+k16]  = acc[5+M];
-        #pragma unroll
-        for (int M = 0; M < 5; ++M) L[792+M*32+16+k16] = acc[8+M];
-      }
-    } else {
-      if (lane < 16) {
-        L[56+k16] = acc[0];
-        #pragma unroll
-        for (int M = 0; M < 3; ++M) L[312+M*40+24+k16] = acc[1+M];
-        #pragma unroll
-        for (int M = 0; M < 5; ++M) L[432+M*72+56+k16] = acc[4+M];
-      }
-    }
-    __syncthreads();
-    const float4* Ls = (const float4*)L;
-    float4* xd = (float4*)(xout + a*952);
-    for (int i = tix; i < 238; i += 256) xd[i] = Ls[i];
-  }
-
-  if constexpr (MODE == 2) {
-    if (wv == 0) {
-      if (lane < 32) {
-        L[k32] = acc[4]*inv[k32];
-        if (k32 < 24) {
-          L[32+k32] = acc[11]*inv[32+k32];
-          #pragma unroll
-          for (int M = 0; M < 3; ++M) L[72+M*80+k32]     = acc[5+M]*inv[72+k32];
-          #pragma unroll
-          for (int M = 0; M < 3; ++M) L[72+M*80+24+k32]  = acc[8+M]*inv[96+k32];
-          #pragma unroll
-          for (int M = 0; M < 3; ++M) L[312+M*40+k32]    = acc[12+M]*inv[152+k32];
-          #pragma unroll
-          for (int M = 0; M < 5; ++M) L[432+M*72+16+k32] = acc[15+M]*inv[208+k32];
-        }
-      }
-    } else if (wv == 1) {
-      if (lane < 16) {
-        #pragma unroll
-        for (int M = 0; M < 5; ++M) L[432+M*72+k16]    = acc[5+M]*inv[192+k16];
-        #pragma unroll
-        for (int M = 0; M < 3; ++M) L[72+M*80+48+k16]  = acc[10+M]*inv[120+k16];
-        #pragma unroll
-        for (int M = 0; M < 5; ++M) L[792+M*32+k16]    = acc[13+M]*inv[264+k16];
-      }
-    } else if (wv == 2) {
-      if (lane < 16) {
-        #pragma unroll
-        for (int M = 0; M < 5; ++M) L[432+M*72+40+k16] = acc[0+M]*inv[232+k16];
-        #pragma unroll
-        for (int M = 0; M < 3; ++M) L[72+M*80+64+k16]  = acc[5+M]*inv[136+k16];
-        #pragma unroll
-        for (int M = 0; M < 5; ++M) L[792+M*32+16+k16] = acc[8+M]*inv[280+k16];
-      }
-    } else {
-      if (lane < 16) {
-        L[56+k16] = acc[0]*inv[56+k16];
-        #pragma unroll
-        for (int M = 0; M < 3; ++M) L[312+M*40+24+k16] = acc[1+M]*inv[176+k16];
-        #pragma unroll
-        for (int M = 0; M < 5; ++M) L[432+M*72+56+k16] = acc[4+M]*inv[248+k16];
-      }
-    }
-    __syncthreads();
-    int t = threadIdx.x;
-    float y2[5] = {0.f,0.f,0.f,0.f,0.f};
-    for (int tau = t; tau < 336; tau += 256) {
-      int ls = 0;
-      while (tau >= c_cum[ls+1]) ++ls;
-      int rem = tau - c_cum[ls];
-      int kn = c_kout[ls], fin = c_fin[ls];
-      int M = rem / kn, ko = rem - M*kn;
-      const T* W = (const T*)lp.W[ls];
-      float y = ldv((const T*)lp.B[ls], ko);
-      const float* xv = &L[c_xb[ls] + M*fin];
-      for (int f = 0; f < fin; ++f) y = fmaf(xv[f], ldv(W, f*kn+ko), y);
-      stv(out, c_yoff[ls] + (a*c_Ms[ls] + M)*kn + ko, y);
-      y2[ls] += y*y;
-    }
-    #pragma unroll
-    for (int i = 0; i < 5; ++i) {
-      y2[i] += __shfl_xor(y2[i], 1);  y2[i] += __shfl_xor(y2[i], 2);
-      y2[i] += __shfl_xor(y2[i], 4);  y2[i] += __shfl_xor(y2[i], 8);
-      y2[i] += __shfl_xor(y2[i], 16); y2[i] += __shfl_xor(y2[i], 32);
-    }
-    if (lane == 0) {
-      #pragma unroll
-      for (int i = 0; i < 5; ++i) red[wv][i] = y2[i];
-    }
-    __syncthreads();
-    if (t == 0) {
-      #pragma unroll
-      for (int i = 0; i < 5; ++i)
-        atomicAdd(&s2p[i*64 + ab], red[0][i]+red[1][i]+red[2][i]+red[3][i]);
-    }
-  }
-}
-
-template<typename T>
-__global__ __launch_bounds__(256) void k_lin(
-    const float* __restrict__ xg, const float* __restrict__ inv,
-    LinP lp, T* __restrict__ out, float* __restrict__ s2p,
-    const int* __restrict__ flag)
-{
-  if (flag[0] != dtid<T>()) return;
-  int a = blockIdx.x;
-  int t = threadIdx.x;
-  __shared__ float L[952];
-  for (int i = t; i < 952; i += 256) {
-    int ch;
-    if      (i < 72)  ch = i;
-    else if (i < 312) ch = 72  + (i-72)  % 80;
-    else if (i < 432) ch = 152 + (i-312) % 40;
-    else if (i < 792) ch = 192 + (i-432) % 72;
-    else              ch = 264 + (i-792) % 32;
-    L[i] = xg[a*952 + i] * inv[ch];
-  }
-  __syncthreads();
-  float y2[5] = {0.f,0.f,0.f,0.f,0.f};
-  for (int tau = t; tau < 336; tau += 256) {
-    int ls = 0;
-    while (tau >= c_cum[ls+1]) ++ls;
-    int rem = tau - c_cum[ls];
-    int kn = c_kout[ls], fin = c_fin[ls];
-    int M = rem / kn, ko = rem - M*kn;
-    const T* W = (const T*)lp.W[ls];
-    float y = ldv((const T*)lp.B[ls], ko);
-    const float* xv = &L[c_xb[ls] + M*fin];
-    for (int f = 0; f < fin; ++f) y = fmaf(xv[f], ldv(W, f*kn+ko), y);
-    stv(out, c_yoff[ls] + (a*c_Ms[ls] + M)*kn + ko, y);
-    y2[ls] += y*y;
-  }
-  __shared__ float red[4][5];
-  #pragma unroll
-  for (int i = 0; i < 5; ++i) {
-    y2[i] += __shfl_xor(y2[i], 1);  y2[i] += __shfl_xor(y2[i], 2);
-    y2[i] += __shfl_xor(y2[i], 4);  y2[i] += __shfl_xor(y2[i], 8);
-    y2[i] += __shfl_xor(y2[i], 16); y2[i] += __shfl_xor(y2[i], 32);
-  }
-  if ((t & 63) == 0) {
-    #pragma unroll
-    for (int i = 0; i < 5; ++i) red[t>>6][i] = y2[i];
-  }
-  __syncthreads();
-  if (t == 0) {
-    #pragma unroll
-    for (int i = 0; i < 5; ++i)
-      atomicAdd(&s2p[i*64 + (a & 63)], red[0][i]+red[1][i]+red[2][i]+red[3][i]);
   }
 }
 
@@ -752,7 +831,7 @@
 
 template<typename T>
 static void launch_chain(void* const* d_in, T* out, float* wsf, int* wsi,
-                         Ptrs15 cg, LinP lp, bool big, hipStream_t stream) {
+                         Ptrs15 cg, LinP lp, bool strm, hipStream_t stream) {
   const T* rb0 = (const T*)d_in[0];
   const T* rb1 = (const T*)d_in[1];
   const T* rb2 = (const T*)d_in[2];
@@ -763,24 +842,32 @@
   const T* f0  = (const T*)d_in[7];
   const T* f1  = (const T*)d_in[8];
   const T* f2  = (const T*)d_in[9];
+  const int* centers   = (const int*)d_in[35];
   const int* neighbors = (const int*)d_in[36];
   const int* flag = wsi + IFLAG;
+  T* erec = (T*)(wsf + SEREC);
 
   k_cg<T><<<3, 256, 0, stream>>>(cg, wsf, flag);
-  if (big) {
-    k_main<T,0><<<N_ATOMS, 256, 0, stream>>>(rb0, rb1, rb2, sh0, sh1, sh2, emb, f0, f1, f2,
-        neighbors, wsi+IOFFS, wsi+IELIST, wsf+SCG, wsf+SS1P, nullptr, nullptr,
-        wsf+SXACC, lp, out, flag);
+  if (strm) {
+    k_pack<T><<<2048, 256, 0, stream>>>(rb0, rb1, rb2, sh0, sh1, sh2,
+        centers, neighbors, wsi+IOFFS, wsi+ICURS, (int2*)(wsi+IELIST), erec, flag);
+    k_main<T,3><<<2500, 256, 0, stream>>>(rb0, rb1, rb2, sh0, sh1, sh2, emb, f0, f1, f2,
+        neighbors, wsi+IOFFS, wsi+IELIST, erec, wsf+SCG, wsf+SS1P, nullptr, nullptr,
+        lp, out, flag);
     k_red1<<<296, 64, 0, stream>>>(wsf+SS1P, wsf+SINV);
-    k_lin<T><<<N_ATOMS, 256, 0, stream>>>(wsf+SXACC, wsf+SINV, lp, out, wsf+SS2P, flag);
+    k_main<T,4><<<2500, 256, 0, stream>>>(rb0, rb1, rb2, sh0, sh1, sh2, emb, f0, f1, f2,
+        neighbors, wsi+IOFFS, wsi+IELIST, erec, wsf+SCG, nullptr, wsf+SINV, wsf+SS2P,
+        lp, out, flag);
   } else {
-    k_main<T,1><<<N_ATOMS, 256, 0, stream>>>(rb0, rb1, rb2, sh0, sh1, sh2, emb, f0, f1, f2,
-        neighbors, wsi+IOFFS, wsi+IELIST, wsf+SCG, wsf+SS1P, nullptr, nullptr,
-        nullptr, lp, out, flag);
+    k_scatterT<T><<<(N_EDGES+255)/256, 256, 0, stream>>>(centers, wsi+IOFFS,
+        wsi+ICURS, wsi+IELIST, flag);
+    k_main<T,1><<<2500, 256, 0, stream>>>(rb0, rb1, rb2, sh0, sh1, sh2, emb, f0, f1, f2,
+        neighbors, wsi+IOFFS, wsi+IELIST, nullptr, wsf+SCG, wsf+SS1P, nullptr, nullptr,
+        lp, out, flag);
     k_red1<<<296, 64, 0, stream>>>(wsf+SS1P, wsf+SINV);
-    k_main<T,2><<<N_ATOMS, 256, 0, stream>>>(rb0, rb1, rb2, sh0, sh1, sh2, emb, f0, f1, f2,
-        neighbors, wsi+IOFFS, wsi+IELIST, wsf+SCG, nullptr, wsf+SINV, wsf+SS2P,
-        nullptr, lp, out, flag);
+    k_main<T,2><<<2500, 256, 0, stream>>>(rb0, rb1, rb2, sh0, sh1, sh2, emb, f0, f1, f2,
+        neighbors, wsi+IOFFS, wsi+IELIST, nullptr, wsf+SCG, nullptr, wsf+SINV, wsf+SS2P,
+        lp, out, flag);
   }
   k_red2<<<5, 64, 0, stream>>>(wsf+SS2P, wsf+SWS2);
   k_scale<T><<<(3360000+255)/256, 256, 0, stream>>>(wsf+SWS2, out, flag);
@@ -792,8 +879,11 @@
   float* wsf = (float*)d_ws;
   int*   wsi = (int*)(wsf + SINTS);
   const int* centers   = (const int*)d_in[35];
-  const int* neighbors = (const int*)d_in[36];
-  bool big = ws_size >= (size_t)BIG_FLOATS * 4;
+
+  size_t need_bf16 = (size_t)SEREC*4 + (size_t)N_EDGES*REC*2 + 256;
+  size_t need_f32  = (size_t)SEREC*4 + (size_t)N_EDGES*REC*4 + 256;
+  bool strm_bf16 = ws_size >= need_bf16;
+  bool strm_f32  = ws_size >= need_f32;
 
   int know = -1;
   if (in_sizes) {
@@ -821,13 +911,7 @@
                                   (const unsigned short*)d_in[6]);
   k_hist<<<(N_EDGES+255)/256, 256, 0, stream>>>(centers, wsi+ICOUNT);
   k_scan<<<1, 1024, 0, stream>>>(wsi+ICOUNT, wsi+IOFFS);
-  if (big) {
-    k_scatter2<<<(N_EDGES+255)/256, 256, 0, stream>>>(centers, neighbors, wsi+IOFFS,
-                                                      wsi+ICURS, (int2*)(wsi+IELIST));
-  } else {
-    k_scatter<<<(N_EDGES+255)/256, 256, 0, stream>>>(centers, wsi+IOFFS, wsi+ICURS, wsi+IELIST);
-  }
-
-  if (know != 1) launch_chain<bf16 >(d_in, (bf16*)d_out,  wsf, wsi, cg, lp, big, stream);
-  if (know != 0) launch_chain<float>(d_in, (float*)d_out, wsf, wsi, cg, lp, big, stream);
-}
+
+  if (know != 1) launch_chain<bf16 >(d_in, (bf16*)d_out,  wsf, wsi, cg, lp, strm_bf16, stream);
+  if (know != 0) launch_chain<float>(d_in, (float*)d_out, wsf, wsi, cg, lp, strm_f32, stream);
+}
```

New measurement: 755.7 us. +47.0%, slower.
